# Optimization experiments

Measured on AMD Instinct MI355X. Metric: run time of the kernel, lower is better.

## Reference

```python
import jax, jax.numpy as jnp
import numpy as np

V = 32000   # vocab_size
D = 1024    # dim
NH = 16     # n_heads
HD = 64     # head_dim
L = 2       # n_layers
E = 8       # n_experts
K = 2       # n_active_experts
H = 2048    # expert_dim
B = 2
T = 1024
EPS = 1e-6
THETA = 10000.0
STD = 0.02


def rmsnorm(x, w):
    rms = jax.lax.rsqrt(jnp.mean(x * x, axis=-1, keepdims=True) + EPS)
    return x * rms * w


def rope_cos_sin(t_len):
    inv = 1.0 / (THETA ** (jnp.arange(0, HD, 2, dtype=jnp.float32) / HD))
    t = jnp.arange(t_len, dtype=jnp.float32)
    f = jnp.outer(t, inv)  # [T, HD//2]
    return jnp.cos(f), jnp.sin(f)


def apply_rope(x, cos, sin):
    # x: [B, T, NH, HD]; complex rotation on interleaved (even, odd) pairs
    xr = x[..., 0::2]
    xi = x[..., 1::2]
    c = cos[None, :, None, :]
    s = sin[None, :, None, :]
    out_r = xr * c - xi * s
    out_i = xr * s + xi * c
    return jnp.stack([out_r, out_i], axis=-1).reshape(x.shape)


def setup_inputs() -> dict:
    key = jax.random.key(0)
    ks = jax.random.split(key, 13)
    n = lambda k, shp: (jax.random.normal(k, shp, dtype=jnp.float32) * STD)
    return {
        "tokens": jax.random.randint(ks[0], (B, T), 0, V, dtype=jnp.int64)
                   if jax.config.jax_enable_x64 else
                   jax.random.randint(ks[0], (B, T), 0, V, dtype=jnp.int32),
        "emb": n(ks[1], (V, D)),            # tied embedding / output projection
        "attn_norm_w": jnp.ones((L, D), jnp.float32),
        "wq": n(ks[2], (L, D, D)),
        "wk": n(ks[3], (L, D, D)),
        "wv": n(ks[4], (L, D, D)),
        "wo": n(ks[5], (L, D, D)),
        "ffn_norm_w": jnp.ones((L, D), jnp.float32),
        "gate_w": n(ks[6], (L, D, E)),
        "w1": n(ks[7], (L, E, D, H)),
        "w2": n(ks[8], (L, E, H, D)),
        "w3": n(ks[9], (L, E, D, H)),
        "final_norm_w": jnp.ones((D,), jnp.float32),
    }


def reference(tokens, emb, attn_norm_w, wq, wk, wv, wo, ffn_norm_w,
              gate_w, w1, w2, w3, final_norm_w):
    b, t = tokens.shape
    h = emb[tokens]                                     # [B,T,D]
    cos, sin = rope_cos_sin(t)
    mask = jnp.where(jnp.tril(jnp.ones((t, t), bool)), 0.0, -jnp.inf)
    scale = 1.0 / np.sqrt(HD).astype(np.float32)
    aux_total = jnp.float32(0.0)

    for l in range(L):
        x = h
        # --- attention ---
        hn = rmsnorm(x, attn_norm_w[l])
        q = (hn @ wq[l]).reshape(b, t, NH, HD)
        k = (hn @ wk[l]).reshape(b, t, NH, HD)
        v = (hn @ wv[l]).reshape(b, t, NH, HD)
        q = apply_rope(q, cos, sin)
        k = apply_rope(k, cos, sin)
        scores = jnp.einsum('bqhd,bkhd->bhqk', q, k) * scale + mask
        attn = jax.nn.softmax(scores, axis=-1)
        o = jnp.einsum('bhqk,bkhd->bqhd', attn, v).reshape(b, t, D) @ wo[l]
        x = x + o
        # --- MoE ---
        xf = rmsnorm(x, ffn_norm_w[l]).reshape(-1, D)   # [N,D]
        gate_logits = xf @ gate_w[l]                    # [N,E]
        probs = jax.nn.softmax(gate_logits, axis=-1)
        vals, idx = jax.lax.top_k(probs, K)             # [N,K]
        w = vals / (jnp.sum(vals, axis=-1, keepdims=True) + 1e-8)
        oh = jax.nn.one_hot(idx, E, dtype=jnp.float32)  # [N,K,E]
        combine = jnp.sum(oh * w[..., None], axis=1)    # [N,E]
        tokens_per_expert = oh.sum(axis=1).mean(axis=0)
        aux_total = aux_total + E * jnp.sum(tokens_per_expert * probs.mean(axis=0))
        h1 = jnp.einsum('nd,edh->neh', xf, w1[l])
        h3 = jnp.einsum('nd,edh->neh', xf, w3[l])
        eo = jnp.einsum('neh,ehd->ned', jax.nn.silu(h1) * h3, w2[l])
        moe_out = jnp.einsum('ned,ne->nd', eo, combine).reshape(b, t, D)
        h = x + moe_out

    logits = rmsnorm(h, final_norm_w) @ emb.T           # [B,T,V]
    return logits, aux_total
```

## Files before the change

kernel.cpp:

```cpp
#include <hip/hip_runtime.h>
#include <hip/hip_bf16.h>
#include <math.h>

#define D_MODEL 1024
#define NHEADS  16
#define HDIM    64
#define NEXP    8
#define FFH     2048
#define BATCH   2
#define SEQ     1024
#define NTOK    2048
#define VOCAB   32000
#define LDSS    40

typedef __attribute__((ext_vector_type(4))) float f32x4;
typedef __attribute__((ext_vector_type(2))) float f32x2;
typedef __attribute__((ext_vector_type(8))) __bf16 bf16x8;
typedef __attribute__((ext_vector_type(4))) unsigned short u16x4;

__device__ __forceinline__ unsigned short f2bf(float f) {
    union { float f; unsigned u; } v; v.f = f;
    unsigned r = v.u + 0x7FFFu + ((v.u >> 16) & 1u);
    return (unsigned short)(r >> 16);
}
__device__ __forceinline__ float bf2f(unsigned short u) {
    union { unsigned u; float f; } v; v.u = ((unsigned)u) << 16; return v.f;
}
__device__ __forceinline__ void split3(float x, unsigned short& h, unsigned short& m, unsigned short& l) {
    h = f2bf(x);
    float r1 = x - bf2f(h);
    m = f2bf(r1);
    float r2 = r1 - bf2f(m);
    l = f2bf(r2);
}
__device__ __forceinline__ void split3t(float x, unsigned short& h, unsigned short& m, unsigned short& l) {
    union { float f; unsigned u; } a; a.f = x;
    h = (unsigned short)(a.u >> 16);
    float r1 = x - bf2f(h);
    union { float f; unsigned u; } b; b.f = r1;
    m = (unsigned short)(b.u >> 16);
    float r2 = r1 - bf2f(m);
    l = f2bf(r2);
}

#define MFMA(a, b, c) __builtin_amdgcn_mfma_f32_16x16x32_bf16((a), (b), (c), 0, 0, 0)

#define PSA ((long)NTOK * D_MODEL)
#define PSW ((long)D_MODEL * D_MODEL)

__global__ __launch_bounds__(256) void rmsnorm_kernel(const float* __restrict__ x,
    const float* __restrict__ wt, unsigned short* __restrict__ out3)
{
    __shared__ float red[4];
    int n = blockIdx.x;
    int c = threadIdx.x << 2;
    f32x4 v = *(const f32x4*)(x + (long)n*D_MODEL + c);
    float ss = v.x*v.x + v.y*v.y + v.z*v.z + v.w*v.w;
    #pragma unroll
    for (int dd = 32; dd; dd >>= 1) ss += __shfl_xor(ss, dd);
    if ((threadIdx.x & 63) == 0) red[threadIdx.x >> 6] = ss;
    __syncthreads();
    float tot = red[0] + red[1] + red[2] + red[3];
    float rms = rsqrtf(tot * (1.f / D_MODEL) + 1e-6f);
    f32x4 wv = *(const f32x4*)(wt + c);
    f32x4 o = v * rms;
    o = o * wv;
    u16x4 hv, mv, lv;
    #pragma unroll
    for (int j = 0; j < 4; j++) { unsigned short h,m,l; split3(o[j],h,m,l); hv[j]=h; mv[j]=m; lv[j]=l; }
    long idx = (long)n*D_MODEL + c;
    *(u16x4*)(out3 + 0*PSA + idx) = hv;
    *(u16x4*)(out3 + 1*PSA + idx) = mv;
    *(u16x4*)(out3 + 2*PSA + idx) = lv;
}

__global__ __launch_bounds__(256) void wsplitT_kernel(
    const float* __restrict__ wqs, const float* __restrict__ wks, const float* __restrict__ wvs,
    unsigned short* __restrict__ oq, unsigned short* __restrict__ ok, unsigned short* __restrict__ ov)
{
    __shared__ float t[64][65];
    int k0 = blockIdx.x*64, n0 = blockIdx.y*64, z = blockIdx.z;
    const float* src = (z==0) ? wqs : (z==1) ? wks : wvs;
    unsigned short* dst = (z==0) ? oq : (z==1) ? ok : ov;
    int tid = threadIdx.x;
    int a = tid & 63, g = tid >> 6;
    #pragma unroll 4
    for (int i = 0; i < 16; i++) {
        int k = g*16 + i;
        t[k][a] = src[(long)(k0+k)*D_MODEL + n0 + a];
    }
    __syncthreads();
    #pragma unroll 4
    for (int i = 0; i < 16; i++) {
        int n = g*16 + i;
        float v = t[a][n];
        unsigned short h,m,l; split3(v,h,m,l);
        long idx = (long)(n0+n)*D_MODEL + k0 + a;
        dst[0*PSW + idx] = h;
        dst[1*PSW + idx] = m;
        dst[2*PSW + idx] = l;
    }
}

__global__ __launch_bounds__(256, 4) void qkv_kernel(
    const unsigned short* __restrict__ A3,
    const unsigned short* __restrict__ Wq3, const unsigned short* __restrict__ Wk3,
    const unsigned short* __restrict__ Wv3,
    float* __restrict__ qf, float* __restrict__ kf, float* __restrict__ vf)
{
    __shared__ __align__(16) unsigned short As[3][64*LDSS];
    __shared__ __align__(16) unsigned short Bs[3][64*LDSS];
    int z = blockIdx.z;
    const unsigned short* B3 = (z==0) ? Wq3 : (z==1) ? Wk3 : Wv3;
    float* out = (z==0) ? qf : (z==1) ? kf : vf;
    int n0 = blockIdx.x*64, m0 = blockIdx.y*64;
    int tid = threadIdx.x, w = tid >> 6, lane = tid & 63;
    int wm = (w >> 1)*32, wn = (w & 1)*32;
    int lr = lane & 15, lg = lane >> 4;
    f32x4 zero = {0.f,0.f,0.f,0.f};
    f32x4 acc[2][2];
    #pragma unroll
    for (int mi = 0; mi < 2; mi++)
        #pragma unroll
        for (int ni = 0; ni < 2; ni++) acc[mi][ni] = zero;
    int rb = tid >> 3, kc = (tid & 7) << 2;

    for (int k0 = 0; k0 < D_MODEL; k0 += 32) {
        #pragma unroll
        for (int p = 0; p < 2; p++) {
            int r = p*32 + rb;
            #pragma unroll
            for (int s = 0; s < 3; s++) {
                *(u16x4*)&As[s][r*LDSS + kc] = *(const u16x4*)(A3 + s*PSA + (long)(m0+r)*D_MODEL + k0 + kc);
                *(u16x4*)&Bs[s][r*LDSS + kc] = *(const u16x4*)(B3 + s*PSW + (long)(n0+r)*D_MODEL + k0 + kc);
            }
        }
        __syncthreads();
        bf16x8 bf[3][2];
        #pragma unroll
        for (int s = 0; s < 3; s++)
            #pragma unroll
            for (int ni = 0; ni < 2; ni++)
                bf[s][ni] = *(const bf16x8*)&Bs[s][(wn + ni*16 + lr)*LDSS + lg*8];
        #pragma unroll
        for (int mi = 0; mi < 2; mi++) {
            bf16x8 ah = *(const bf16x8*)&As[0][(wm + mi*16 + lr)*LDSS + lg*8];
            bf16x8 am = *(const bf16x8*)&As[1][(wm + mi*16 + lr)*LDSS + lg*8];
            bf16x8 al = *(const bf16x8*)&As[2][(wm + mi*16 + lr)*LDSS + lg*8];
            #pragma unroll
            for (int ni = 0; ni < 2; ni++) {
                acc[mi][ni] = MFMA(ah, bf[0][ni], acc[mi][ni]);
                acc[mi][ni] = MFMA(ah, bf[1][ni], acc[mi][ni]);
                acc[mi][ni] = MFMA(am, bf[0][ni], acc[mi][ni]);
                acc[mi][ni] = MFMA(ah, bf[2][ni], acc[mi][ni]);
                acc[mi][ni] = MFMA(am, bf[1][ni], acc[mi][ni]);
                acc[mi][ni] = MFMA(al, bf[0][ni], acc[mi][ni]);
            }
        }
        __syncthreads();
    }
    #pragma unroll
    for (int mi = 0; mi < 2; mi++)
        #pragma unroll
        for (int r = 0; r < 4; r++) {
            long row = m0 + wm + mi*16 + lg*4 + r;
            #pragma unroll
            for (int ni = 0; ni < 2; ni++) {
                int col = n0 + wn + ni*16 + lr;
                out[row*D_MODEL + col] = acc[mi][ni][r];
            }
        }
}

__global__ __launch_bounds__(256, 3) void wo_kernel(
    const float* __restrict__ A, const float* __restrict__ B, float* h)
{
    __shared__ __align__(16) unsigned short As[3][64*LDSS];
    __shared__ __align__(16) unsigned short Bs[3][64*LDSS];
    int n0 = blockIdx.x*64, m0 = blockIdx.y*64;
    int tid = threadIdx.x, w = tid >> 6, lane = tid & 63;
    int wm = (w >> 1)*32, wn = (w & 1)*32;
    int lr = lane & 15, lg = lane >> 4;
    f32x4 zero = {0.f,0.f,0.f,0.f};
    f32x4 acc[2][2];
    #pragma unroll
    for (int mi = 0; mi < 2; mi++)
        #pragma unroll
        for (int ni = 0; ni < 2; ni++) acc[mi][ni] = zero;
    int rb = tid >> 3, kc = (tid & 7) << 2;
    int nb = (tid & 31) << 1, kb = (tid >> 5) << 2;

    f32x4 pAv[2];
    f32x2 pBv[4];
    #pragma unroll
    for (int p = 0; p < 2; p++)
        pAv[p] = *(const f32x4*)(A + (long)(m0 + p*32 + rb)*D_MODEL + kc);
    #pragma unroll
    for (int i = 0; i < 4; i++)
        pBv[i] = *(const f32x2*)(B + (long)(kb + i)*D_MODEL + n0 + nb);

    for (int k0 = 0; k0 < D_MODEL; k0 += 32) {
        int kn = k0 + 32;
        #pragma unroll
        for (int p = 0; p < 2; p++) {
            int r = p*32 + rb;
            u16x4 hv, mv, lv;
            #pragma unroll
            for (int j = 0; j < 4; j++) { unsigned short h,m,l; split3t(pAv[p][j],h,m,l); hv[j]=h; mv[j]=m; lv[j]=l; }
            *(u16x4*)&As[0][r*LDSS + kc] = hv;
            *(u16x4*)&As[1][r*LDSS + kc] = mv;
            *(u16x4*)&As[2][r*LDSS + kc] = lv;
        }
        #pragma unroll
        for (int i = 0; i < 2; i++) {
            int r = nb + i;
            u16x4 hv, mv, lv;
            unsigned short h,m,l;
            split3t(pBv[0][i],h,m,l); hv[0]=h; mv[0]=m; lv[0]=l;
            split3t(pBv[1][i],h,m,l); hv[1]=h; mv[1]=m; lv[1]=l;
            split3t(pBv[2][i],h,m,l); hv[2]=h; mv[2]=m; lv[2]=l;
            split3t(pBv[3][i],h,m,l); hv[3]=h; mv[3]=m; lv[3]=l;
            *(u16x4*)&Bs[0][r*LDSS + kb] = hv;
            *(u16x4*)&Bs[1][r*LDSS + kb] = mv;
            *(u16x4*)&Bs[2][r*LDSS + kb] = lv;
        }
        if (kn < D_MODEL) {
            #pragma unroll
            for (int p = 0; p < 2; p++)
                pAv[p] = *(const f32x4*)(A + (long)(m0 + p*32 + rb)*D_MODEL + kn + kc);
            #pragma unroll
            for (int i = 0; i < 4; i++)
                pBv[i] = *(const f32x2*)(B + (long)(kn + kb + i)*D_MODEL + n0 + nb);
        }
        __syncthreads();
        bf16x8 bf[3][2];
        #pragma unroll
        for (int s = 0; s < 3; s++)
            #pragma unroll
            for (int ni = 0; ni < 2; ni++)
                bf[s][ni] = *(const bf16x8*)&Bs[s][(wn + ni*16 + lr)*LDSS + lg*8];
        #pragma unroll
        for (int mi = 0; mi < 2; mi++) {
            bf16x8 ah = *(const bf16x8*)&As[0][(wm + mi*16 + lr)*LDSS + lg*8];
            bf16x8 am = *(const bf16x8*)&As[1][(wm + mi*16 + lr)*LDSS + lg*8];
            bf16x8 al = *(const bf16x8*)&As[2][(wm + mi*16 + lr)*LDSS + lg*8];
            #pragma unroll
            for (int ni = 0; ni < 2; ni++) {
                acc[mi][ni] = MFMA(ah, bf[0][ni], acc[mi][ni]);
                acc[mi][ni] = MFMA(ah, bf[1][ni], acc[mi][ni]);
                acc[mi][ni] = MFMA(am, bf[0][ni], acc[mi][ni]);
                acc[mi][ni] = MFMA(ah, bf[2][ni], acc[mi][ni]);
                acc[mi][ni] = MFMA(am, bf[1][ni], acc[mi][ni]);
                acc[mi][ni] = MFMA(al, bf[0][ni], acc[mi][ni]);
            }
        }
        __syncthreads();
    }
    #pragma unroll
    for (int mi = 0; mi < 2; mi++)
        #pragma unroll
        for (int r = 0; r < 4; r++) {
            long row = m0 + wm + mi*16 + lg*4 + r;
            #pragma unroll
            for (int ni = 0; ni < 2; ni++) {
                int col = n0 + wn + ni*16 + lr;
                h[row*D_MODEL + col] += acc[mi][ni][r];
            }
        }
}

template<int SPLIT>
__global__ __launch_bounds__(256, 3) void moe13_kernel(
    const unsigned short* __restrict__ A3, const float* __restrict__ W1,
    const float* __restrict__ W3, float* __restrict__ G,
    const int* __restrict__ rowidx, const int* __restrict__ counts,
    const int* __restrict__ offsets)
{
    __shared__ __align__(16) unsigned short As[SPLIT][64*LDSS];
    __shared__ __align__(16) unsigned short Bs[SPLIT][128*LDSS];
    int e = blockIdx.z;
    int cnt = counts[e], off = offsets[e];
    int n0 = blockIdx.x*128, m0 = blockIdx.y*64;
    if (m0 >= cnt) return;
    const float* b1p = W1 + (long)e * (D_MODEL*FFH);
    const float* b3p = W3 + (long)e * (D_MODEL*FFH);
    int tid = threadIdx.x, w = tid >> 6, lane = tid & 63;
    int wm = (w >> 1)*32, wn = (w & 1)*64;
    int lr = lane & 15, lg = lane >> 4;
    f32x4 zero = {0.f,0.f,0.f,0.f};
    f32x4 a1[2][4], a3[2][4];
    #pragma unroll
    for (int mi = 0; mi < 2; mi++)
        #pragma unroll
        for (int ni = 0; ni < 4; ni++) { a1[mi][ni] = zero; a3[mi][ni] = zero; }
    int rb = tid >> 3, kc = (tid & 7) << 2;

    long arow[2]; int av[2];
    #pragma unroll
    for (int p = 0; p < 2; p++) {
        int r = p*32 + rb;
        av[p] = (m0 + r < cnt) ? 1 : 0;
        arow[p] = av[p] ? (long)rowidx[off + m0 + r] : 0;
    }
    u16x4 z4 = {0,0,0,0};

    for (int k0 = 0; k0 < D_MODEL; k0 += 32) {
        #pragma unroll
        for (int p = 0; p < 2; p++) {
            int r = p*32 + rb;
            #pragma unroll
            for (int s = 0; s < SPLIT; s++)
                *(u16x4*)&As[s][r*LDSS + kc] = av[p] ?
                    *(const u16x4*)(A3 + s*PSA + arow[p]*D_MODEL + k0 + kc) : z4;
        }
        #pragma unroll
        for (int pass = 0; pass < 2; pass++) {
            const float* bp = pass ? b3p : b1p;
            f32x4 c0 = *(const f32x4*)(bp + (long)(k0+kc+0)*FFH + n0 + rb*4);
            f32x4 c1 = *(const f32x4*)(bp + (long)(k0+kc+1)*FFH + n0 + rb*4);
            f32x4 c2 = *(const f32x4*)(bp + (long)(k0+kc+2)*FFH + n0 + rb*4);
            f32x4 c3 = *(const f32x4*)(bp + (long)(k0+kc+3)*FFH + n0 + rb*4);
            #pragma unroll
            for (int i = 0; i < 4; i++) {
                int r = rb*4 + i;
                if (SPLIT == 3) {
                    u16x4 hv, mv, lv;
                    unsigned short h,m,l;
                    split3t(c0[i],h,m,l); hv[0]=h; mv[0]=m; lv[0]=l;
                    split3t(c1[i],h,m,l); hv[1]=h; mv[1]=m; lv[1]=l;
                    split3t(c2[i],h,m,l); hv[2]=h; mv[2]=m; lv[2]=l;
                    split3t(c3[i],h,m,l); hv[3]=h; mv[3]=m; lv[3]=l;
                    *(u16x4*)&Bs[0][r*LDSS + kc] = hv;
                    *(u16x4*)&Bs[1][r*LDSS + kc] = mv;
                    *(u16x4*)&Bs[2][r*LDSS + kc] = lv;
                } else {
                    u16x4 hv = {f2bf(c0[i]), f2bf(c1[i]), f2bf(c2[i]), f2bf(c3[i])};
                    *(u16x4*)&Bs[0][r*LDSS + kc] = hv;
                }
            }
            __syncthreads();
            bf16x8 bf[SPLIT][4];
            #pragma unroll
            for (int s = 0; s < SPLIT; s++)
                #pragma unroll
                for (int ni = 0; ni < 4; ni++)
                    bf[s][ni] = *(const bf16x8*)&Bs[s][(wn + ni*16 + lr)*LDSS + lg*8];
            #pragma unroll
            for (int mi = 0; mi < 2; mi++) {
                bf16x8 ah = *(const bf16x8*)&As[0][(wm + mi*16 + lr)*LDSS + lg*8];
                #pragma unroll
                for (int ni = 0; ni < 4; ni++) {
                    f32x4 a = pass ? a3[mi][ni] : a1[mi][ni];
                    a = MFMA(ah, bf[0][ni], a);
                    if (SPLIT == 3) {
                        bf16x8 am = *(const bf16x8*)&As[1][(wm + mi*16 + lr)*LDSS + lg*8];
                        bf16x8 al = *(const bf16x8*)&As[2][(wm + mi*16 + lr)*LDSS + lg*8];
                        a = MFMA(ah, bf[1][ni], a);
                        a = MFMA(am, bf[0][ni], a);
                        a = MFMA(ah, bf[2][ni], a);
                        a = MFMA(am, bf[1][ni], a);
                        a = MFMA(al, bf[0][ni], a);
                    }
                    if (pass) a3[mi][ni] = a; else a1[mi][ni] = a;
                }
            }
            __syncthreads();
        }
    }
    #pragma unroll
    for (int mi = 0; mi < 2; mi++)
        #pragma unroll
        for (int r = 0; r < 4; r++) {
            int rowl = wm + mi*16 + lg*4 + r;
            if (m0 + rowl < cnt) {
                long crow = off + m0 + rowl;
                #pragma unroll
                for (int ni = 0; ni < 4; ni++) {
                    int col = n0 + wn + ni*16 + lr;
                    float v1 = a1[mi][ni][r];
                    float v3 = a3[mi][ni][r];
                    G[crow*FFH + col] = (v1 / (1.f + expf(-v1))) * v3;
                }
            }
        }
}

template<int SPLIT>
__global__ __launch_bounds__(256, 4) void w2_kernel(
    const float* __restrict__ G, const float* __restrict__ W2, float* h,
    const int* __restrict__ rowidx, const float* __restrict__ wrow,
    const int* __restrict__ counts, const int* __restrict__ offsets)
{
    __shared__ __align__(16) unsigned short As[SPLIT][64*LDSS];
    __shared__ __align__(16) unsigned short Bs[SPLIT][64*LDSS];
    int e = blockIdx.z;
    int cnt = counts[e], off = offsets[e];
    int n0 = blockIdx.x*64, m0 = blockIdx.y*64;
    if (m0 >= cnt) return;
    const float* bp = W2 + (long)e * (FFH*D_MODEL);
    int tid = threadIdx.x, w = tid >> 6, lane = tid & 63;
    int wm = (w >> 1)*32, wn = (w & 1)*32;
    int lr = lane & 15, lg = lane >> 4;
    f32x4 zero = {0.f,0.f,0.f,0.f};
    f32x4 acc[2][2];
    #pragma unroll
    for (int mi = 0; mi < 2; mi++)
        #pragma unroll
        for (int ni = 0; ni < 2; ni++) acc[mi][ni] = zero;
    int rb = tid >> 3, kc = (tid & 7) << 2;
    int nb = (tid & 31) << 1, kb = (tid >> 5) << 2;

    int av[2];
    #pragma unroll
    for (int p = 0; p < 2; p++) av[p] = (m0 + p*32 + rb < cnt) ? 1 : 0;
    f32x4 pG[2];
    f32x2 pW[4];
    #pragma unroll
    for (int p = 0; p < 2; p++)
        pG[p] = av[p] ? *(const f32x4*)(G + (long)(off + m0 + p*32 + rb)*FFH + kc) : zero;
    #pragma unroll
    for (int i = 0; i < 4; i++)
        pW[i] = *(const f32x2*)(bp + (long)(kb + i)*D_MODEL + n0 + nb);

    for (int k0 = 0; k0 < FFH; k0 += 32) {
        int kn = k0 + 32;
        #pragma unroll
        for (int p = 0; p < 2; p++) {
            int r = p*32 + rb;
            if (SPLIT == 3) {
                u16x4 hv, mv, lv;
                #pragma unroll
                for (int j = 0; j < 4; j++) { unsigned short h,m,l; split3t(pG[p][j],h,m,l); hv[j]=h; mv[j]=m; lv[j]=l; }
                *(u16x4*)&As[0][r*LDSS + kc] = hv;
                *(u16x4*)&As[1][r*LDSS + kc] = mv;
                *(u16x4*)&As[2][r*LDSS + kc] = lv;
            } else {
                u16x4 hv;
                #pragma unroll
                for (int j = 0; j < 4; j++) hv[j] = f2bf(pG[p][j]);
                *(u16x4*)&As[0][r*LDSS + kc] = hv;
            }
        }
        #pragma unroll
        for (int i = 0; i < 2; i++) {
            int r = nb + i;
            if (SPLIT == 3) {
                u16x4 hv, mv, lv;
                unsigned short h,m,l;
                split3t(pW[0][i],h,m,l); hv[0]=h; mv[0]=m; lv[0]=l;
                split3t(pW[1][i],h,m,l); hv[1]=h; mv[1]=m; lv[1]=l;
                split3t(pW[2][i],h,m,l); hv[2]=h; mv[2]=m; lv[2]=l;
                split3t(pW[3][i],h,m,l); hv[3]=h; mv[3]=m; lv[3]=l;
                *(u16x4*)&Bs[0][r*LDSS + kb] = hv;
                *(u16x4*)&Bs[1][r*LDSS + kb] = mv;
                *(u16x4*)&Bs[2][r*LDSS + kb] = lv;
            } else {
                u16x4 hv = {f2bf(pW[0][i]), f2bf(pW[1][i]), f2bf(pW[2][i]), f2bf(pW[3][i])};
                *(u16x4*)&Bs[0][r*LDSS + kb] = hv;
            }
        }
        if (kn < FFH) {
            #pragma unroll
            for (int p = 0; p < 2; p++)
                pG[p] = av[p] ? *(const f32x4*)(G + (long)(off + m0 + p*32 + rb)*FFH + kn + kc) : zero;
            #pragma unroll
            for (int i = 0; i < 4; i++)
                pW[i] = *(const f32x2*)(bp + (long)(kn + kb + i)*D_MODEL + n0 + nb);
        }
        __syncthreads();
        bf16x8 bf[SPLIT][2];
        #pragma unroll
        for (int s = 0; s < SPLIT; s++)
            #pragma unroll
            for (int ni = 0; ni < 2; ni++)
                bf[s][ni] = *(const bf16x8*)&Bs[s][(wn + ni*16 + lr)*LDSS + lg*8];
        #pragma unroll
        for (int mi = 0; mi < 2; mi++) {
            bf16x8 ah = *(const bf16x8*)&As[0][(wm + mi*16 + lr)*LDSS + lg*8];
            #pragma unroll
            for (int ni = 0; ni < 2; ni++) {
                acc[mi][ni] = MFMA(ah, bf[0][ni], acc[mi][ni]);
                if (SPLIT == 3) {
                    bf16x8 am = *(const bf16x8*)&As[1][(wm + mi*16 + lr)*LDSS + lg*8];
                    bf16x8 al = *(const bf16x8*)&As[2][(wm + mi*16 + lr)*LDSS + lg*8];
                    acc[mi][ni] = MFMA(ah, bf[1][ni], acc[mi][ni]);
                    acc[mi][ni] = MFMA(am, bf[0][ni], acc[mi][ni]);
                    acc[mi][ni] = MFMA(ah, bf[2][ni], acc[mi][ni]);
                    acc[mi][ni] = MFMA(am, bf[1][ni], acc[mi][ni]);
                    acc[mi][ni] = MFMA(al, bf[0][ni], acc[mi][ni]);
                }
            }
        }
        __syncthreads();
    }
    #pragma unroll
    for (int mi = 0; mi < 2; mi++)
        #pragma unroll
        for (int r = 0; r < 4; r++) {
            int rowl = wm + mi*16 + lg*4 + r;
            if (m0 + rowl < cnt) {
                long crow = off + m0 + rowl;
                long n = rowidx[crow];
                float wgt = wrow[crow];
                #pragma unroll
                for (int ni = 0; ni < 2; ni++) {
                    int col = n0 + wn + ni*16 + lr;
                    atomicAdd(&h[n*D_MODEL + col], wgt * acc[mi][ni][r]);
                }
            }
        }
}

__global__ __launch_bounds__(256) void attn_kernel(
    const float* __restrict__ q, const float* __restrict__ k,
    const float* __restrict__ v, float* __restrict__ att)
{
    __shared__ __align__(16) unsigned short Qs[3][64*72];
    __shared__ __align__(16) unsigned short KP[3][2560];
    __shared__ __align__(16) unsigned short Vt[3][2560];

    int qt = blockIdx.x, bh = blockIdx.y;
    int b = bh >> 4, hh = bh & 15;
    int tid = threadIdx.x, w = tid >> 6, lane = tid & 63;
    int lr = lane & 15, lg = lane >> 4;
    int lrow = tid >> 4;
    int lcol = (tid & 15) << 2;

    const float* qbase = q + ((long)(b*SEQ + qt*64) * D_MODEL + hh*64);
    #pragma unroll
    for (int p = 0; p < 4; p++) {
        int r = p*16 + lrow;
        f32x4 vv = *(const f32x4*)(qbase + (long)r * D_MODEL + lcol);
        #pragma unroll
        for (int jj = 0; jj < 4; jj++) {
            unsigned short h,m,l; split3t(vv[jj],h,m,l);
            Qs[0][r*72 + lcol + jj] = h;
            Qs[1][r*72 + lcol + jj] = m;
            Qs[2][r*72 + lcol + jj] = l;
        }
    }

    f32x4 zero = {0.f,0.f,0.f,0.f};
    f32x4 oacc[4] = {zero, zero, zero, zero};
    float mrun[4] = {-INFINITY,-INFINITY,-INFINITY,-INFINITY};
    float lrun[4] = {0.f,0.f,0.f,0.f};

    int ntile = 2*qt + 2;
    for (int jt = 0; jt < ntile; jt++) {
        const float* kbase = k + ((long)(b*SEQ + jt*32) * D_MODEL + hh*64);
        const float* vbase = v + ((long)(b*SEQ + jt*32) * D_MODEL + hh*64);
        #pragma unroll
        for (int p = 0; p < 2; p++) {
            int r = p*16 + lrow;
            f32x4 kv4 = *(const f32x4*)(kbase + (long)r * D_MODEL + lcol);
            f32x4 vv4 = *(const f32x4*)(vbase + (long)r * D_MODEL + lcol);
            #pragma unroll
            for (int jj = 0; jj < 4; jj++) {
                unsigned short h,m,l;
                split3t(kv4[jj],h,m,l);
                KP[0][r*72 + lcol + jj] = h;
                KP[1][r*72 + lcol + jj] = m;
                KP[2][r*72 + lcol + jj] = l;
                split3t(vv4[jj],h,m,l);
                Vt[0][(lcol+jj)*40 + r] = h;
                Vt[1][(lcol+jj)*40 + r] = m;
                Vt[2][(lcol+jj)*40 + r] = l;
            }
        }
        __syncthreads();

        f32x4 s[2] = {zero, zero};
        #pragma unroll
        for (int ks = 0; ks < 2; ks++) {
            bf16x8 qh = *(const bf16x8*)&Qs[0][(w*16 + lr)*72 + ks*32 + lg*8];
            bf16x8 qm = *(const bf16x8*)&Qs[1][(w*16 + lr)*72 + ks*32 + lg*8];
            bf16x8 ql = *(const bf16x8*)&Qs[2][(w*16 + lr)*72 + ks*32 + lg*8];
            #pragma unroll
            for (int ni = 0; ni < 2; ni++) {
                bf16x8 kh = *(const bf16x8*)&KP[0][(ni*16 + lr)*72 + ks*32 + lg*8];
                bf16x8 km = *(const bf16x8*)&KP[1][(ni*16 + lr)*72 + ks*32 + lg*8];
                bf16x8 kl = *(const bf16x8*)&KP[2][(ni*16 + lr)*72 + ks*32 + lg*8];
                s[ni] = MFMA(qh, kh, s[ni]);
                s[ni] = MFMA(qh, km, s[ni]);
                s[ni] = MFMA(qm, kh, s[ni]);
                s[ni] = MFMA(qh, kl, s[ni]);
                s[ni] = MFMA(qm, km, s[ni]);
                s[ni] = MFMA(ql, kh, s[ni]);
            }
        }
        __syncthreads();

        #pragma unroll
        for (int r = 0; r < 4; r++) {
            int qg = qt*64 + w*16 + lg*4 + r;
            float mx = -INFINITY;
            #pragma unroll
            for (int ni = 0; ni < 2; ni++) {
                int kg = jt*32 + ni*16 + lr;
                float val = s[ni][r] * 0.125f;
                if (kg > qg) val = -INFINITY;
                s[ni][r] = val;
                mx = fmaxf(mx, val);
            }
            #pragma unroll
            for (int dd = 1; dd < 16; dd <<= 1)
                mx = fmaxf(mx, __shfl_xor(mx, dd));
            float mnew  = fmaxf(mrun[r], mx);
            float alpha = expf(mrun[r] - mnew);
            float ps = 0.f;
            #pragma unroll
            for (int ni = 0; ni < 2; ni++) {
                float pv = expf(s[ni][r] - mnew);
                s[ni][r] = pv;
                ps += pv;
            }
            #pragma unroll
            for (int dd = 1; dd < 16; dd <<= 1)
                ps += __shfl_xor(ps, dd);
            lrun[r] = lrun[r] * alpha + ps;
            mrun[r] = mnew;
            #pragma unroll
            for (int d = 0; d < 4; d++) oacc[d][r] *= alpha;
            int prow = w*16 + lg*4 + r;
            #pragma unroll
            for (int ni = 0; ni < 2; ni++) {
                unsigned short h,m,l; split3t(s[ni][r],h,m,l);
                KP[0][prow*40 + ni*16 + lr] = h;
                KP[1][prow*40 + ni*16 + lr] = m;
                KP[2][prow*40 + ni*16 + lr] = l;
            }
        }
        {
            bf16x8 ph = *(const bf16x8*)&KP[0][(w*16 + lr)*40 + lg*8];
            bf16x8 pm = *(const bf16x8*)&KP[1][(w*16 + lr)*40 + lg*8];
            bf16x8 pl = *(const bf16x8*)&KP[2][(w*16 + lr)*40 + lg*8];
            #pragma unroll
            for (int ni = 0; ni < 4; ni++) {
                bf16x8 vh = *(const bf16x8*)&Vt[0][(ni*16 + lr)*40 + lg*8];
                bf16x8 vm = *(const bf16x8*)&Vt[1][(ni*16 + lr)*40 + lg*8];
                bf16x8 vl = *(const bf16x8*)&Vt[2][(ni*16 + lr)*40 + lg*8];
                oacc[ni] = MFMA(ph, vh, oacc[ni]);
                oacc[ni] = MFMA(ph, vm, oacc[ni]);
                oacc[ni] = MFMA(pm, vh, oacc[ni]);
                oacc[ni] = MFMA(ph, vl, oacc[ni]);
                oacc[ni] = MFMA(pm, vm, oacc[ni]);
                oacc[ni] = MFMA(pl, vh, oacc[ni]);
            }
        }
        __syncthreads();
    }
    float* obase = att + ((long)(b*SEQ + qt*64) * D_MODEL + hh*64);
    #pragma unroll
    for (int r = 0; r < 4; r++) {
        float inv = 1.f / lrun[r];
        #pragma unroll
        for (int ni = 0; ni < 4; ni++)
            obase[(long)(w*16 + lg*4 + r) * D_MODEL + ni*16 + lr] = oacc[ni][r] * inv;
    }
}

__global__ __launch_bounds__(256) void logits_kernel(
    const unsigned short* __restrict__ A0, const float* __restrict__ Bmat, float* __restrict__ C)
{
    __shared__ __align__(16) unsigned short As[128*LDSS];
    __shared__ __align__(16) unsigned short Bs[128*LDSS];
    int n0 = blockIdx.y * 128;
    int m0 = blockIdx.x * 128;
    int tid = threadIdx.x, w = tid >> 6, lane = tid & 63;
    int wm = (w >> 1)*64, wn = (w & 1)*64;
    int lr = lane & 15, lg = lane >> 4;
    f32x4 zero = {0.f,0.f,0.f,0.f};
    f32x4 acc[4][4];
    #pragma unroll
    for (int mi = 0; mi < 4; mi++)
        #pragma unroll
        for (int ni = 0; ni < 4; ni++) acc[mi][ni] = zero;
    int rb = tid >> 3, kc = (tid & 7) << 2;
    for (int k0 = 0; k0 < D_MODEL; k0 += 32) {
        #pragma unroll
        for (int p = 0; p < 4; p++) {
            int r = p*32 + rb;
            *(u16x4*)&As[r*LDSS + kc] = *(const u16x4*)(A0 + (long)(m0+r)*D_MODEL + k0 + kc);
            f32x4 vv = *(const f32x4*)(Bmat + (long)(n0+r)*D_MODEL + k0 + kc);
            u16x4 hv;
            #pragma unroll
            for (int j = 0; j < 4; j++) hv[j] = f2bf(vv[j]);
            *(u16x4*)&Bs[r*LDSS + kc] = hv;
        }
        __syncthreads();
        bf16x8 bfv[4], af[4];
        #pragma unroll
        for (int ni = 0; ni < 4; ni++)
            bfv[ni] = *(const bf16x8*)&Bs[(wn + ni*16 + lr)*LDSS + lg*8];
        #pragma unroll
        for (int mi = 0; mi < 4; mi++)
            af[mi] = *(const bf16x8*)&As[(wm + mi*16 + lr)*LDSS + lg*8];
        #pragma unroll
        for (int mi = 0; mi < 4; mi++)
            #pragma unroll
            for (int ni = 0; ni < 4; ni++)
                acc[mi][ni] = MFMA(af[mi], bfv[ni], acc[mi][ni]);
        __syncthreads();
    }
    #pragma unroll
    for (int mi = 0; mi < 4; mi++)
        #pragma unroll
        for (int r = 0; r < 4; r++) {
            long row = m0 + wm + mi*16 + lg*4 + r;
            #pragma unroll
            for (int ni = 0; ni < 4; ni++) {
                int col = n0 + wn + ni*16 + lr;
                C[row*VOCAB + col] = acc[mi][ni][r];
            }
        }
}

__global__ __launch_bounds__(256) void embed_kernel(const int* __restrict__ tok,
    const float* __restrict__ emb, float* __restrict__ h)
{
    int n = blockIdx.x;
    int c = threadIdx.x << 2;
    long t = tok[n];
    *(f32x4*)(h + (long)n*D_MODEL + c) = *(const f32x4*)(emb + t*D_MODEL + c);
}

__global__ __launch_bounds__(256) void ropetab_kernel(float* __restrict__ tab)
{
    int idx = blockIdx.x * 256 + threadIdx.x;
    if (idx >= SEQ * 32) return;
    int t = idx >> 5, i = idx & 31;
    double inv = pow(10000.0, -(double)(2*i) / 64.0);
    double ang = (double)t * inv;
    tab[idx*2]   = (float)cos(ang);
    tab[idx*2+1] = (float)sin(ang);
}

__global__ __launch_bounds__(256) void rope_kernel(float* __restrict__ q, float* __restrict__ kk,
    const float* __restrict__ tab)
{
    int gid = blockIdx.x * 256 + threadIdx.x;
    if (gid >= NTOK * 512) return;
    int n   = gid >> 9;
    int rem = gid & 511;
    int hh  = rem >> 5;
    int i   = rem & 31;
    int t   = n & (SEQ - 1);
    float cs = tab[(t*32 + i)*2];
    float sn = tab[(t*32 + i)*2 + 1];
    long base = (long)n * D_MODEL + hh*64 + 2*i;
    float qr = q[base], qi = q[base+1];
    q[base]   = qr*cs - qi*sn;
    q[base+1] = qr*sn + qi*cs;
    float kr = kk[base], ki = kk[base+1];
    kk[base]   = kr*cs - ki*sn;
    kk[base+1] = kr*sn + ki*cs;
}

__global__ __launch_bounds__(64) void gate_kernel(const unsigned short* __restrict__ xf3,
    const float* __restrict__ gw, int* __restrict__ counts,
    int* __restrict__ eid, float* __restrict__ wts, float* __restrict__ pbuf)
{
    int n = blockIdx.x;
    int lane = threadIdx.x;
    float acc[8] = {0,0,0,0,0,0,0,0};
    for (int d0 = lane*4; d0 < D_MODEL; d0 += 256) {
        long idx = (long)n*D_MODEL + d0;
        u16x4 xh = *(const u16x4*)(xf3 + 0*PSA + idx);
        u16x4 xm = *(const u16x4*)(xf3 + 1*PSA + idx);
        u16x4 xl = *(const u16x4*)(xf3 + 2*PSA + idx);
        #pragma unroll
        for (int j = 0; j < 4; j++) {
            float xv = bf2f(xh[j]) + bf2f(xm[j]) + bf2f(xl[j]);
            const float* g = gw + (d0+j) * 8;
            #pragma unroll
            for (int e = 0; e < 8; e++) acc[e] += xv * g[e];
        }
    }
    #pragma unroll
    for (int e = 0; e < 8; e++) {
        #pragma unroll
        for (int dd = 32; dd; dd >>= 1) acc[e] += __shfl_xor(acc[e], dd);
    }
    if (lane == 0) {
        float mx = acc[0];
        #pragma unroll
        for (int e = 1; e < 8; e++) mx = fmaxf(mx, acc[e]);
        float pe[8], ssum = 0.f;
        #pragma unroll
        for (int e = 0; e < 8; e++) { pe[e] = expf(acc[e] - mx); ssum += pe[e]; }
        float sinv = 1.f / ssum;
        #pragma unroll
        for (int e = 0; e < 8; e++) { pe[e] *= sinv; pbuf[n*8 + e] = pe[e]; }
        int e1 = 0;
        #pragma unroll
        for (int e = 1; e < 8; e++) if (pe[e] > pe[e1]) e1 = e;
        int e2 = -1;
        #pragma unroll
        for (int e = 0; e < 8; e++) if (e != e1 && (e2 < 0 || pe[e] > pe[e2])) e2 = e;
        float v1 = pe[e1], v2 = pe[e2];
        float wsum = v1 + v2 + 1e-8f;
        eid[n*2] = e1; eid[n*2+1] = e2;
        wts[n*2] = v1 / wsum; wts[n*2+1] = v2 / wsum;
        atomicAdd(counts + e1, 1);
        atomicAdd(counts + e2, 1);
    }
}

__global__ __launch_bounds__(64) void scan_kernel(const int* __restrict__ counts,
    int* __restrict__ offs, int* __restrict__ cursor,
    const float* __restrict__ pbuf, float* __restrict__ aux)
{
    int t = threadIdx.x;
    int e = t & 7, c = t >> 3;
    float s = 0.f;
    for (int n = 0; n < NTOK/8; n++)
        s += pbuf[(c*(NTOK/8) + n)*8 + e];
    #pragma unroll
    for (int dd = 8; dd < 64; dd <<= 1) s += __shfl_xor(s, dd);
    __shared__ float red[8];
    if (t < 8) red[t] = s;
    __syncthreads();
    if (t == 0) {
        int o = 0; float a = 0.f;
        for (int k = 0; k < 8; k++) {
            offs[k] = o; cursor[k] = o; o += counts[k];
            a += (float)counts[k] * red[k];
        }
        aux[0] += 8.f * a / ((float)NTOK * (float)NTOK);
    }
}

__global__ __launch_bounds__(256) void assign_kernel(const int* __restrict__ eid,
    const float* __restrict__ wts, int* __restrict__ cursor,
    int* __restrict__ rowidx, float* __restrict__ wrow)
{
    int n = blockIdx.x * 256 + threadIdx.x;
    if (n >= NTOK) return;
    #pragma unroll
    for (int s = 0; s < 2; s++) {
        int e = eid[n*2 + s];
        int p = atomicAdd(cursor + e, 1);
        rowidx[p] = n;
        wrow[p] = wts[n*2 + s];
    }
}

__global__ void write_aux_kernel(float* __restrict__ out, const float* __restrict__ aux)
{
    if (threadIdx.x == 0 && blockIdx.x == 0)
        out[(long)NTOK * VOCAB] = aux[0];
}

extern "C" void kernel_launch(void* const* d_in, const int* in_sizes, int n_in,
                              void* d_out, int out_size, void* d_ws, size_t ws_size,
                              hipStream_t stream)
{
    const int*   tokens = (const int*)d_in[0];
    const float* emb    = (const float*)d_in[1];
    const float* anw    = (const float*)d_in[2];
    const float* wq     = (const float*)d_in[3];
    const float* wk     = (const float*)d_in[4];
    const float* wv     = (const float*)d_in[5];
    const float* wo     = (const float*)d_in[6];
    const float* fnw    = (const float*)d_in[7];
    const float* gw     = (const float*)d_in[8];
    const float* w1     = (const float*)d_in[9];
    const float* w2     = (const float*)d_in[10];
    const float* w3     = (const float*)d_in[11];
    const float* finw   = (const float*)d_in[12];
    float* out = (float*)d_out;

    char* W = (char*)d_ws;
    const size_t MB = 1024u * 1024u;
    int*   counts = (int*)(W + 0);
    int*   offs   = (int*)(W + 64);
    int*   cursor = (int*)(W + 128);
    float* aux    = (float*)(W + 192);
    int*   eid    = (int*)(W + 4096);
    float* wts    = (float*)(W + 4096 + 16384);
    int*   rowix  = (int*)(W + 4096 + 32768);
    float* wrow   = (float*)(W + 4096 + 49152);
    float* pbuf   = (float*)(W + 4096 + 65536);
    float* rtab   = (float*)(W + 4096 + 131072 + 65536);
    float*          h    = (float*)(W + 1*MB);
    unsigned short* hn3  = (unsigned short*)(W + 9*MB);
    float*          qf   = (float*)(W + 21*MB);
    float*          kf   = (float*)(W + 29*MB);
    float*          vf   = (float*)(W + 37*MB);
    unsigned short* wq3  = (unsigned short*)(W + 45*MB);
    unsigned short* wk3  = (unsigned short*)(W + 51*MB);
    unsigned short* wv3  = (unsigned short*)(W + 57*MB);
    float*          att  = (float*)(W + 45*MB);
    float*          g    = (float*)(W + 21*MB);

    hipMemsetAsync(W, 0, 256, stream);
    ropetab_kernel<<<(SEQ*32 + 255)/256, 256, 0, stream>>>(rtab);
    embed_kernel<<<NTOK, 256, 0, stream>>>(tokens, emb, h);

    for (int l = 0; l < 2; l++) {
        const float* wql = wq + (size_t)l*D_MODEL*D_MODEL;
        const float* wkl = wk + (size_t)l*D_MODEL*D_MODEL;
        const float* wvl = wv + (size_t)l*D_MODEL*D_MODEL;
        const float* wol = wo + (size_t)l*D_MODEL*D_MODEL;

        rmsnorm_kernel<<<NTOK, 256, 0, stream>>>(h, anw + (size_t)l*D_MODEL, hn3);
        wsplitT_kernel<<<dim3(16, 16, 3), 256, 0, stream>>>(wql, wkl, wvl, wq3, wk3, wv3);
        qkv_kernel<<<dim3(D_MODEL/64, NTOK/64, 3), 256, 0, stream>>>(hn3, wq3, wk3, wv3, qf, kf, vf);
        rope_kernel<<<(NTOK*512 + 255)/256, 256, 0, stream>>>(qf, kf, rtab);
        attn_kernel<<<dim3(SEQ/64, BATCH*NHEADS), 256, 0, stream>>>(qf, kf, vf, att);
        wo_kernel<<<dim3(D_MODEL/64, NTOK/64), 256, 0, stream>>>(att, wol, h);

        rmsnorm_kernel<<<NTOK, 256, 0, stream>>>(h, fnw + (size_t)l*D_MODEL, hn3);
        hipMemsetAsync(W, 0, 160, stream);
        gate_kernel<<<NTOK, 64, 0, stream>>>(hn3, gw + (size_t)l*D_MODEL*NEXP, counts, eid, wts, pbuf);
        scan_kernel<<<1, 64, 0, stream>>>(counts, offs, cursor, pbuf, aux);
        assign_kernel<<<(NTOK + 255)/256, 256, 0, stream>>>(eid, wts, cursor, rowix, wrow);

        const float* w1l = w1 + (size_t)l*NEXP*D_MODEL*FFH;
        const float* w3l = w3 + (size_t)l*NEXP*D_MODEL*FFH;
        const float* w2l = w2 + (size_t)l*NEXP*FFH*D_MODEL;
        dim3 g13(FFH/128, 2*NTOK/64, NEXP);
        dim3 g2d(D_MODEL/64, 2*NTOK/64, NEXP);
        if (l == 0) {
            moe13_kernel<3><<<g13, 256, 0, stream>>>(hn3, w1l, w3l, g, rowix, counts, offs);
            w2_kernel<3><<<g2d, 256, 0, stream>>>(g, w2l, h, rowix, wrow, counts, offs);
        } else {
            moe13_kernel<1><<<g13, 256, 0, stream>>>(hn3, w1l, w3l, g, rowix, counts, offs);
            w2_kernel<1><<<g2d, 256, 0, stream>>>(g, w2l, h, rowix, wrow, counts, offs);
        }
    }

    rmsnorm_kernel<<<NTOK, 256, 0, stream>>>(h, finw, hn3);
    logits_kernel<<<dim3(NTOK/128, VOCAB/128), 256, 0, stream>>>(hn3, emb, out);
    write_aux_kernel<<<1, 1, 0, stream>>>(out, aux);
}
```

Baseline: 1.975 ms.

## Replace 3-way bf16 split GEMMs with scaled 2-way fp16 split

Switches every emulated-fp32 matmul from a three-term bf16 decomposition (six MFMAs per tile) to a two-term scaled fp16 decomposition (three MFMAs per tile). Separate accumulators are rescaled and summed in the epilogue. This cuts MFMA count, LDS footprint and split-operand memory traffic roughly in half. The risk is reduced precision and fp16 range overflow or underflow, since fixed scale factors are assumed for activations and weights.

After: 1.740 ms. -11.9%, faster.

```diff
diff --git a/kernel.cpp b/kernel.cpp
--- a/kernel.cpp
+++ b/kernel.cpp
@@ -15,41 +15,38 @@
 
 typedef __attribute__((ext_vector_type(4))) float f32x4;
 typedef __attribute__((ext_vector_type(2))) float f32x2;
-typedef __attribute__((ext_vector_type(8))) __bf16 bf16x8;
+typedef __attribute__((ext_vector_type(8))) _Float16 f16x8;
 typedef __attribute__((ext_vector_type(4))) unsigned short u16x4;
 
-__device__ __forceinline__ unsigned short f2bf(float f) {
-    union { float f; unsigned u; } v; v.f = f;
-    unsigned r = v.u + 0x7FFFu + ((v.u >> 16) & 1u);
-    return (unsigned short)(r >> 16);
-}
-__device__ __forceinline__ float bf2f(unsigned short u) {
-    union { unsigned u; float f; } v; v.u = ((unsigned)u) << 16; return v.f;
-}
-__device__ __forceinline__ void split3(float x, unsigned short& h, unsigned short& m, unsigned short& l) {
-    h = f2bf(x);
-    float r1 = x - bf2f(h);
-    m = f2bf(r1);
-    float r2 = r1 - bf2f(m);
-    l = f2bf(r2);
-}
-__device__ __forceinline__ void split3t(float x, unsigned short& h, unsigned short& m, unsigned short& l) {
-    union { float f; unsigned u; } a; a.f = x;
-    h = (unsigned short)(a.u >> 16);
-    float r1 = x - bf2f(h);
-    union { float f; unsigned u; } b; b.f = r1;
-    m = (unsigned short)(b.u >> 16);
-    float r2 = r1 - bf2f(m);
-    l = f2bf(r2);
-}
-
-#define MFMA(a, b, c) __builtin_amdgcn_mfma_f32_16x16x32_bf16((a), (b), (c), 0, 0, 0)
+#define TIER    4.8828125e-4f
+#define DESCALE 2.44140625e-4f
+#define INV_S   0.015625f
+#define INV_M   7.62939453125e-6f
+
+__device__ __forceinline__ unsigned short f2h(float x) {
+    _Float16 h = (_Float16)x;
+    union { _Float16 h; unsigned short u; } v; v.h = h; return v.u;
+}
+__device__ __forceinline__ float h2f(unsigned short u) {
+    union { unsigned short u; _Float16 h; } v; v.u = u; return (float)v.h;
+}
+__device__ __forceinline__ void split2h(float x, unsigned short& h, unsigned short& m) {
+    _Float16 hf = (_Float16)(x * 64.f);
+    union { _Float16 h; unsigned short u; } a; a.h = hf;
+    h = a.u;
+    float r = x - (float)hf * INV_S;
+    _Float16 mf = (_Float16)(r * 131072.f);
+    union { _Float16 h; unsigned short u; } b; b.h = mf;
+    m = b.u;
+}
+
+#define MFMAH(a, b, c) __builtin_amdgcn_mfma_f32_16x16x32_f16((a), (b), (c), 0, 0, 0)
 
 #define PSA ((long)NTOK * D_MODEL)
 #define PSW ((long)D_MODEL * D_MODEL)
 
 __global__ __launch_bounds__(256) void rmsnorm_kernel(const float* __restrict__ x,
-    const float* __restrict__ wt, unsigned short* __restrict__ out3)
+    const float* __restrict__ wt, unsigned short* __restrict__ out2)
 {
     __shared__ float red[4];
     int n = blockIdx.x;
@@ -65,13 +62,12 @@
     f32x4 wv = *(const f32x4*)(wt + c);
     f32x4 o = v * rms;
     o = o * wv;
-    u16x4 hv, mv, lv;
-    #pragma unroll
-    for (int j = 0; j < 4; j++) { unsigned short h,m,l; split3(o[j],h,m,l); hv[j]=h; mv[j]=m; lv[j]=l; }
+    u16x4 hv, mv;
+    #pragma unroll
+    for (int j = 0; j < 4; j++) { unsigned short h,m; split2h(o[j],h,m); hv[j]=h; mv[j]=m; }
     long idx = (long)n*D_MODEL + c;
-    *(u16x4*)(out3 + 0*PSA + idx) = hv;
-    *(u16x4*)(out3 + 1*PSA + idx) = mv;
-    *(u16x4*)(out3 + 2*PSA + idx) = lv;
+    *(u16x4*)(out2 + 0*PSA + idx) = hv;
+    *(u16x4*)(out2 + 1*PSA + idx) = mv;
 }
 
 __global__ __launch_bounds__(256) void wsplitT_kernel(
@@ -94,35 +90,34 @@
     for (int i = 0; i < 16; i++) {
         int n = g*16 + i;
         float v = t[a][n];
-        unsigned short h,m,l; split3(v,h,m,l);
+        unsigned short h,m; split2h(v,h,m);
         long idx = (long)(n0+n)*D_MODEL + k0 + a;
         dst[0*PSW + idx] = h;
         dst[1*PSW + idx] = m;
-        dst[2*PSW + idx] = l;
     }
 }
 
 __global__ __launch_bounds__(256, 4) void qkv_kernel(
-    const unsigned short* __restrict__ A3,
-    const unsigned short* __restrict__ Wq3, const unsigned short* __restrict__ Wk3,
-    const unsigned short* __restrict__ Wv3,
+    const unsigned short* __restrict__ A2,
+    const unsigned short* __restrict__ Wq2, const unsigned short* __restrict__ Wk2,
+    const unsigned short* __restrict__ Wv2,
     float* __restrict__ qf, float* __restrict__ kf, float* __restrict__ vf)
 {
-    __shared__ __align__(16) unsigned short As[3][64*LDSS];
-    __shared__ __align__(16) unsigned short Bs[3][64*LDSS];
+    __shared__ __align__(16) unsigned short As[2][64*LDSS];
+    __shared__ __align__(16) unsigned short Bs[2][64*LDSS];
     int z = blockIdx.z;
-    const unsigned short* B3 = (z==0) ? Wq3 : (z==1) ? Wk3 : Wv3;
+    const unsigned short* B2 = (z==0) ? Wq2 : (z==1) ? Wk2 : Wv2;
     float* out = (z==0) ? qf : (z==1) ? kf : vf;
     int n0 = blockIdx.x*64, m0 = blockIdx.y*64;
     int tid = threadIdx.x, w = tid >> 6, lane = tid & 63;
     int wm = (w >> 1)*32, wn = (w & 1)*32;
     int lr = lane & 15, lg = lane >> 4;
     f32x4 zero = {0.f,0.f,0.f,0.f};
-    f32x4 acc[2][2];
+    f32x4 a0[2][2], a1[2][2];
     #pragma unroll
     for (int mi = 0; mi < 2; mi++)
         #pragma unroll
-        for (int ni = 0; ni < 2; ni++) acc[mi][ni] = zero;
+        for (int ni = 0; ni < 2; ni++) { a0[mi][ni] = zero; a1[mi][ni] = zero; }
     int rb = tid >> 3, kc = (tid & 7) << 2;
 
     for (int k0 = 0; k0 < D_MODEL; k0 += 32) {
@@ -130,31 +125,27 @@
         for (int p = 0; p < 2; p++) {
             int r = p*32 + rb;
             #pragma unroll
-            for (int s = 0; s < 3; s++) {
-                *(u16x4*)&As[s][r*LDSS + kc] = *(const u16x4*)(A3 + s*PSA + (long)(m0+r)*D_MODEL + k0 + kc);
-                *(u16x4*)&Bs[s][r*LDSS + kc] = *(const u16x4*)(B3 + s*PSW + (long)(n0+r)*D_MODEL + k0 + kc);
-            }
-        }
-        __syncthreads();
-        bf16x8 bf[3][2];
-        #pragma unroll
-        for (int s = 0; s < 3; s++)
-            #pragma unroll
-            for (int ni = 0; ni < 2; ni++)
-                bf[s][ni] = *(const bf16x8*)&Bs[s][(wn + ni*16 + lr)*LDSS + lg*8];
+            for (int s = 0; s < 2; s++) {
+                *(u16x4*)&As[s][r*LDSS + kc] = *(const u16x4*)(A2 + s*PSA + (long)(m0+r)*D_MODEL + k0 + kc);
+                *(u16x4*)&Bs[s][r*LDSS + kc] = *(const u16x4*)(B2 + s*PSW + (long)(n0+r)*D_MODEL + k0 + kc);
+            }
+        }
+        __syncthreads();
+        f16x8 bh[2], bm[2];
+        #pragma unroll
+        for (int ni = 0; ni < 2; ni++) {
+            bh[ni] = *(const f16x8*)&Bs[0][(wn + ni*16 + lr)*LDSS + lg*8];
+            bm[ni] = *(const f16x8*)&Bs[1][(wn + ni*16 + lr)*LDSS + lg*8];
+        }
         #pragma unroll
         for (int mi = 0; mi < 2; mi++) {
-            bf16x8 ah = *(const bf16x8*)&As[0][(wm + mi*16 + lr)*LDSS + lg*8];
-            bf16x8 am = *(const bf16x8*)&As[1][(wm + mi*16 + lr)*LDSS + lg*8];
-            bf16x8 al = *(const bf16x8*)&As[2][(wm + mi*16 + lr)*LDSS + lg*8];
+            f16x8 ah = *(const f16x8*)&As[0][(wm + mi*16 + lr)*LDSS + lg*8];
+            f16x8 am = *(const f16x8*)&As[1][(wm + mi*16 + lr)*LDSS + lg*8];
             #pragma unroll
             for (int ni = 0; ni < 2; ni++) {
-                acc[mi][ni] = MFMA(ah, bf[0][ni], acc[mi][ni]);
-                acc[mi][ni] = MFMA(ah, bf[1][ni], acc[mi][ni]);
-                acc[mi][ni] = MFMA(am, bf[0][ni], acc[mi][ni]);
-                acc[mi][ni] = MFMA(ah, bf[2][ni], acc[mi][ni]);
-                acc[mi][ni] = MFMA(am, bf[1][ni], acc[mi][ni]);
-                acc[mi][ni] = MFMA(al, bf[0][ni], acc[mi][ni]);
+                a0[mi][ni] = MFMAH(ah, bh[ni], a0[mi][ni]);
+                a1[mi][ni] = MFMAH(ah, bm[ni], a1[mi][ni]);
+                a1[mi][ni] = MFMAH(am, bh[ni], a1[mi][ni]);
             }
         }
         __syncthreads();
@@ -167,7 +158,7 @@
             #pragma unroll
             for (int ni = 0; ni < 2; ni++) {
                 int col = n0 + wn + ni*16 + lr;
-                out[row*D_MODEL + col] = acc[mi][ni][r];
+                out[row*D_MODEL + col] = (a0[mi][ni][r] + a1[mi][ni][r]*TIER) * DESCALE;
             }
         }
 }
@@ -175,18 +166,18 @@
 __global__ __launch_bounds__(256, 3) void wo_kernel(
     const float* __restrict__ A, const float* __restrict__ B, float* h)
 {
-    __shared__ __align__(16) unsigned short As[3][64*LDSS];
-    __shared__ __align__(16) unsigned short Bs[3][64*LDSS];
+    __shared__ __align__(16) unsigned short As[2][64*LDSS];
+    __shared__ __align__(16) unsigned short Bs[2][64*LDSS];
     int n0 = blockIdx.x*64, m0 = blockIdx.y*64;
     int tid = threadIdx.x, w = tid >> 6, lane = tid & 63;
     int wm = (w >> 1)*32, wn = (w & 1)*32;
     int lr = lane & 15, lg = lane >> 4;
     f32x4 zero = {0.f,0.f,0.f,0.f};
-    f32x4 acc[2][2];
+    f32x4 a0[2][2], a1[2][2];
     #pragma unroll
     for (int mi = 0; mi < 2; mi++)
         #pragma unroll
-        for (int ni = 0; ni < 2; ni++) acc[mi][ni] = zero;
+        for (int ni = 0; ni < 2; ni++) { a0[mi][ni] = zero; a1[mi][ni] = zero; }
     int rb = tid >> 3, kc = (tid & 7) << 2;
     int nb = (tid & 31) << 1, kb = (tid >> 5) << 2;
 
@@ -204,25 +195,23 @@
         #pragma unroll
         for (int p = 0; p < 2; p++) {
             int r = p*32 + rb;
-            u16x4 hv, mv, lv;
-            #pragma unroll
-            for (int j = 0; j < 4; j++) { unsigned short h,m,l; split3t(pAv[p][j],h,m,l); hv[j]=h; mv[j]=m; lv[j]=l; }
+            u16x4 hv, mv;
+            #pragma unroll
+            for (int j = 0; j < 4; j++) { unsigned short hh,mm; split2h(pAv[p][j],hh,mm); hv[j]=hh; mv[j]=mm; }
             *(u16x4*)&As[0][r*LDSS + kc] = hv;
             *(u16x4*)&As[1][r*LDSS + kc] = mv;
-            *(u16x4*)&As[2][r*LDSS + kc] = lv;
         }
         #pragma unroll
         for (int i = 0; i < 2; i++) {
             int r = nb + i;
-            u16x4 hv, mv, lv;
-            unsigned short h,m,l;
-            split3t(pBv[0][i],h,m,l); hv[0]=h; mv[0]=m; lv[0]=l;
-            split3t(pBv[1][i],h,m,l); hv[1]=h; mv[1]=m; lv[1]=l;
-            split3t(pBv[2][i],h,m,l); hv[2]=h; mv[2]=m; lv[2]=l;
-            split3t(pBv[3][i],h,m,l); hv[3]=h; mv[3]=m; lv[3]=l;
+            u16x4 hv, mv;
+            unsigned short hh,mm;
+            split2h(pBv[0][i],hh,mm); hv[0]=hh; mv[0]=mm;
+            split2h(pBv[1][i],hh,mm); hv[1]=hh; mv[1]=mm;
+            split2h(pBv[2][i],hh,mm); hv[2]=hh; mv[2]=mm;
+            split2h(pBv[3][i],hh,mm); hv[3]=hh; mv[3]=mm;
             *(u16x4*)&Bs[0][r*LDSS + kb] = hv;
             *(u16x4*)&Bs[1][r*LDSS + kb] = mv;
-            *(u16x4*)&Bs[2][r*LDSS + kb] = lv;
         }
         if (kn < D_MODEL) {
             #pragma unroll
@@ -233,25 +222,21 @@
                 pBv[i] = *(const f32x2*)(B + (long)(kn + kb + i)*D_MODEL + n0 + nb);
         }
         __syncthreads();
-        bf16x8 bf[3][2];
-        #pragma unroll
-        for (int s = 0; s < 3; s++)
-            #pragma unroll
-            for (int ni = 0; ni < 2; ni++)
-                bf[s][ni] = *(const bf16x8*)&Bs[s][(wn + ni*16 + lr)*LDSS + lg*8];
+        f16x8 bh[2], bm[2];
+        #pragma unroll
+        for (int ni = 0; ni < 2; ni++) {
+            bh[ni] = *(const f16x8*)&Bs[0][(wn + ni*16 + lr)*LDSS + lg*8];
+            bm[ni] = *(const f16x8*)&Bs[1][(wn + ni*16 + lr)*LDSS + lg*8];
+        }
         #pragma unroll
         for (int mi = 0; mi < 2; mi++) {
-            bf16x8 ah = *(const bf16x8*)&As[0][(wm + mi*16 + lr)*LDSS + lg*8];
-            bf16x8 am = *(const bf16x8*)&As[1][(wm + mi*16 + lr)*LDSS + lg*8];
-            bf16x8 al = *(const bf16x8*)&As[2][(wm + mi*16 + lr)*LDSS + lg*8];
+            f16x8 ah = *(const f16x8*)&As[0][(wm + mi*16 + lr)*LDSS + lg*8];
+            f16x8 am = *(const f16x8*)&As[1][(wm + mi*16 + lr)*LDSS + lg*8];
             #pragma unroll
             for (int ni = 0; ni < 2; ni++) {
-                acc[mi][ni] = MFMA(ah, bf[0][ni], acc[mi][ni]);
-                acc[mi][ni] = MFMA(ah, bf[1][ni], acc[mi][ni]);
-                acc[mi][ni] = MFMA(am, bf[0][ni], acc[mi][ni]);
-                acc[mi][ni] = MFMA(ah, bf[2][ni], acc[mi][ni]);
-                acc[mi][ni] = MFMA(am, bf[1][ni], acc[mi][ni]);
-                acc[mi][ni] = MFMA(al, bf[0][ni], acc[mi][ni]);
+                a0[mi][ni] = MFMAH(ah, bh[ni], a0[mi][ni]);
+                a1[mi][ni] = MFMAH(ah, bm[ni], a1[mi][ni]);
+                a1[mi][ni] = MFMAH(am, bh[ni], a1[mi][ni]);
             }
         }
         __syncthreads();
@@ -264,36 +249,30 @@
             #pragma unroll
             for (int ni = 0; ni < 2; ni++) {
                 int col = n0 + wn + ni*16 + lr;
-                h[row*D_MODEL + col] += acc[mi][ni][r];
-            }
-        }
-}
-
-template<int SPLIT>
+                h[row*D_MODEL + col] += (a0[mi][ni][r] + a1[mi][ni][r]*TIER) * DESCALE;
+            }
+        }
+}
+
+template<int SPL>
 __global__ __launch_bounds__(256, 3) void moe13_kernel(
-    const unsigned short* __restrict__ A3, const float* __restrict__ W1,
+    const unsigned short* __restrict__ A2, const float* __restrict__ W1,
     const float* __restrict__ W3, float* __restrict__ G,
     const int* __restrict__ rowidx, const int* __restrict__ counts,
     const int* __restrict__ offsets)
 {
-    __shared__ __align__(16) unsigned short As[SPLIT][64*LDSS];
-    __shared__ __align__(16) unsigned short Bs[SPLIT][128*LDSS];
+    __shared__ __align__(16) unsigned short As[SPL][64*LDSS];
+    __shared__ __align__(16) unsigned short Bs[SPL][128*LDSS];
+    const int P1 = (SPL == 2) ? 1 : 0;
     int e = blockIdx.z;
     int cnt = counts[e], off = offsets[e];
     int n0 = blockIdx.x*128, m0 = blockIdx.y*64;
     if (m0 >= cnt) return;
-    const float* b1p = W1 + (long)e * (D_MODEL*FFH);
-    const float* b3p = W3 + (long)e * (D_MODEL*FFH);
     int tid = threadIdx.x, w = tid >> 6, lane = tid & 63;
     int wm = (w >> 1)*32, wn = (w & 1)*64;
     int lr = lane & 15, lg = lane >> 4;
+    int rb = tid >> 3, kc = (tid & 7) << 2;
     f32x4 zero = {0.f,0.f,0.f,0.f};
-    f32x4 a1[2][4], a3[2][4];
-    #pragma unroll
-    for (int mi = 0; mi < 2; mi++)
-        #pragma unroll
-        for (int ni = 0; ni < 4; ni++) { a1[mi][ni] = zero; a3[mi][ni] = zero; }
-    int rb = tid >> 3, kc = (tid & 7) << 2;
 
     long arow[2]; int av[2];
     #pragma unroll
@@ -303,19 +282,26 @@
         arow[p] = av[p] ? (long)rowidx[off + m0 + r] : 0;
     }
     u16x4 z4 = {0,0,0,0};
-
-    for (int k0 = 0; k0 < D_MODEL; k0 += 32) {
-        #pragma unroll
-        for (int p = 0; p < 2; p++) {
-            int r = p*32 + rb;
-            #pragma unroll
-            for (int s = 0; s < SPLIT; s++)
-                *(u16x4*)&As[s][r*LDSS + kc] = av[p] ?
-                    *(const u16x4*)(A3 + s*PSA + arow[p]*D_MODEL + k0 + kc) : z4;
-        }
-        #pragma unroll
-        for (int pass = 0; pass < 2; pass++) {
-            const float* bp = pass ? b3p : b1p;
+    f32x4 sl[2][4];
+
+    #pragma unroll
+    for (int mat = 0; mat < 2; mat++) {
+        const float* bp = (mat ? W3 : W1) + (long)e * (D_MODEL*FFH);
+        f32x4 a0[2][4], a1t[2][4];
+        #pragma unroll
+        for (int mi = 0; mi < 2; mi++)
+            #pragma unroll
+            for (int ni = 0; ni < 4; ni++) { a0[mi][ni] = zero; a1t[mi][ni] = zero; }
+
+        for (int k0 = 0; k0 < D_MODEL; k0 += 32) {
+            #pragma unroll
+            for (int p = 0; p < 2; p++) {
+                int r = p*32 + rb;
+                #pragma unroll
+                for (int s = 0; s < SPL; s++)
+                    *(u16x4*)&As[s][r*LDSS + kc] = av[p] ?
+                        *(const u16x4*)(A2 + s*PSA + arow[p]*D_MODEL + k0 + kc) : z4;
+            }
             f32x4 c0 = *(const f32x4*)(bp + (long)(k0+kc+0)*FFH + n0 + rb*4);
             f32x4 c1 = *(const f32x4*)(bp + (long)(k0+kc+1)*FFH + n0 + rb*4);
             f32x4 c2 = *(const f32x4*)(bp + (long)(k0+kc+2)*FFH + n0 + rb*4);
@@ -323,76 +309,86 @@
             #pragma unroll
             for (int i = 0; i < 4; i++) {
                 int r = rb*4 + i;
-                if (SPLIT == 3) {
-                    u16x4 hv, mv, lv;
-                    unsigned short h,m,l;
-                    split3t(c0[i],h,m,l); hv[0]=h; mv[0]=m; lv[0]=l;
-                    split3t(c1[i],h,m,l); hv[1]=h; mv[1]=m; lv[1]=l;
-                    split3t(c2[i],h,m,l); hv[2]=h; mv[2]=m; lv[2]=l;
-                    split3t(c3[i],h,m,l); hv[3]=h; mv[3]=m; lv[3]=l;
+                if (SPL == 2) {
+                    u16x4 hv, mv;
+                    unsigned short hh,mm;
+                    split2h(c0[i],hh,mm); hv[0]=hh; mv[0]=mm;
+                    split2h(c1[i],hh,mm); hv[1]=hh; mv[1]=mm;
+                    split2h(c2[i],hh,mm); hv[2]=hh; mv[2]=mm;
+                    split2h(c3[i],hh,mm); hv[3]=hh; mv[3]=mm;
                     *(u16x4*)&Bs[0][r*LDSS + kc] = hv;
-                    *(u16x4*)&Bs[1][r*LDSS + kc] = mv;
-                    *(u16x4*)&Bs[2][r*LDSS + kc] = lv;
+                    *(u16x4*)&Bs[P1][r*LDSS + kc] = mv;
                 } else {
-                    u16x4 hv = {f2bf(c0[i]), f2bf(c1[i]), f2bf(c2[i]), f2bf(c3[i])};
+                    u16x4 hv = {f2h(c0[i]), f2h(c1[i]), f2h(c2[i]), f2h(c3[i])};
                     *(u16x4*)&Bs[0][r*LDSS + kc] = hv;
                 }
             }
             __syncthreads();
-            bf16x8 bf[SPLIT][4];
-            #pragma unroll
-            for (int s = 0; s < SPLIT; s++)
-                #pragma unroll
-                for (int ni = 0; ni < 4; ni++)
-                    bf[s][ni] = *(const bf16x8*)&Bs[s][(wn + ni*16 + lr)*LDSS + lg*8];
+            f16x8 bh[4], bm[4];
+            #pragma unroll
+            for (int ni = 0; ni < 4; ni++) {
+                bh[ni] = *(const f16x8*)&Bs[0][(wn + ni*16 + lr)*LDSS + lg*8];
+                if (SPL == 2) bm[ni] = *(const f16x8*)&Bs[P1][(wn + ni*16 + lr)*LDSS + lg*8];
+            }
             #pragma unroll
             for (int mi = 0; mi < 2; mi++) {
-                bf16x8 ah = *(const bf16x8*)&As[0][(wm + mi*16 + lr)*LDSS + lg*8];
+                f16x8 ah = *(const f16x8*)&As[0][(wm + mi*16 + lr)*LDSS + lg*8];
                 #pragma unroll
                 for (int ni = 0; ni < 4; ni++) {
-                    f32x4 a = pass ? a3[mi][ni] : a1[mi][ni];
-                    a = MFMA(ah, bf[0][ni], a);
-                    if (SPLIT == 3) {
-                        bf16x8 am = *(const bf16x8*)&As[1][(wm + mi*16 + lr)*LDSS + lg*8];
-                        bf16x8 al = *(const bf16x8*)&As[2][(wm + mi*16 + lr)*LDSS + lg*8];
-                        a = MFMA(ah, bf[1][ni], a);
-                        a = MFMA(am, bf[0][ni], a);
-                        a = MFMA(ah, bf[2][ni], a);
-                        a = MFMA(am, bf[1][ni], a);
-                        a = MFMA(al, bf[0][ni], a);
+                    a0[mi][ni] = MFMAH(ah, bh[ni], a0[mi][ni]);
+                    if (SPL == 2) {
+                        f16x8 am = *(const f16x8*)&As[P1][(wm + mi*16 + lr)*LDSS + lg*8];
+                        a1t[mi][ni] = MFMAH(ah, bm[ni], a1t[mi][ni]);
+                        a1t[mi][ni] = MFMAH(am, bh[ni], a1t[mi][ni]);
                     }
-                    if (pass) a3[mi][ni] = a; else a1[mi][ni] = a;
                 }
             }
             __syncthreads();
         }
-    }
-    #pragma unroll
-    for (int mi = 0; mi < 2; mi++)
-        #pragma unroll
-        for (int r = 0; r < 4; r++) {
-            int rowl = wm + mi*16 + lg*4 + r;
-            if (m0 + rowl < cnt) {
-                long crow = off + m0 + rowl;
+        if (mat == 0) {
+            #pragma unroll
+            for (int mi = 0; mi < 2; mi++)
                 #pragma unroll
                 for (int ni = 0; ni < 4; ni++) {
-                    int col = n0 + wn + ni*16 + lr;
-                    float v1 = a1[mi][ni][r];
-                    float v3 = a3[mi][ni][r];
-                    G[crow*FFH + col] = (v1 / (1.f + expf(-v1))) * v3;
+                    f32x4 v = (SPL == 2) ? (a0[mi][ni] + a1t[mi][ni]*TIER)*DESCALE
+                                         : a0[mi][ni]*INV_S;
+                    #pragma unroll
+                    for (int r = 0; r < 4; r++) {
+                        float s = v[r];
+                        v[r] = s / (1.f + expf(-s));
+                    }
+                    sl[mi][ni] = v;
                 }
-            }
-        }
-}
-
-template<int SPLIT>
+        } else {
+            #pragma unroll
+            for (int mi = 0; mi < 2; mi++)
+                #pragma unroll
+                for (int r = 0; r < 4; r++) {
+                    int rowl = wm + mi*16 + lg*4 + r;
+                    if (m0 + rowl < cnt) {
+                        long crow = off + m0 + rowl;
+                        #pragma unroll
+                        for (int ni = 0; ni < 4; ni++) {
+                            int col = n0 + wn + ni*16 + lr;
+                            float v3 = (SPL == 2) ? (a0[mi][ni][r] + a1t[mi][ni][r]*TIER)*DESCALE
+                                                  : a0[mi][ni][r]*INV_S;
+                            G[crow*FFH + col] = sl[mi][ni][r] * v3;
+                        }
+                    }
+                }
+        }
+    }
+}
+
+template<int SPL>
 __global__ __launch_bounds__(256, 4) void w2_kernel(
     const float* __restrict__ G, const float* __restrict__ W2, float* h,
     const int* __restrict__ rowidx, const float* __restrict__ wrow,
     const int* __restrict__ counts, const int* __restrict__ offsets)
 {
-    __shared__ __align__(16) unsigned short As[SPLIT][64*LDSS];
-    __shared__ __align__(16) unsigned short Bs[SPLIT][64*LDSS];
+    __shared__ __align__(16) unsigned short As[SPL][64*LDSS];
+    __shared__ __align__(16) unsigned short Bs[SPL][64*LDSS];
+    const int P1 = (SPL == 2) ? 1 : 0;
     int e = blockIdx.z;
     int cnt = counts[e], off = offsets[e];
     int n0 = blockIdx.x*64, m0 = blockIdx.y*64;
@@ -402,11 +398,11 @@
     int wm = (w >> 1)*32, wn = (w & 1)*32;
     int lr = lane & 15, lg = lane >> 4;
     f32x4 zero = {0.f,0.f,0.f,0.f};
-    f32x4 acc[2][2];
+    f32x4 a0[2][2], a1[2][2];
     #pragma unroll
     for (int mi = 0; mi < 2; mi++)
         #pragma unroll
-        for (int ni = 0; ni < 2; ni++) acc[mi][ni] = zero;
+        for (int ni = 0; ni < 2; ni++) { a0[mi][ni] = zero; a1[mi][ni] = zero; }
     int rb = tid >> 3, kc = (tid & 7) << 2;
     int nb = (tid & 31) << 1, kb = (tid >> 5) << 2;
 
@@ -427,35 +423,33 @@
         #pragma unroll
         for (int p = 0; p < 2; p++) {
             int r = p*32 + rb;
-            if (SPLIT == 3) {
-                u16x4 hv, mv, lv;
+            if (SPL == 2) {
+                u16x4 hv, mv;
                 #pragma unroll
-                for (int j = 0; j < 4; j++) { unsigned short h,m,l; split3t(pG[p][j],h,m,l); hv[j]=h; mv[j]=m; lv[j]=l; }
+                for (int j = 0; j < 4; j++) { unsigned short hh,mm; split2h(pG[p][j],hh,mm); hv[j]=hh; mv[j]=mm; }
                 *(u16x4*)&As[0][r*LDSS + kc] = hv;
-                *(u16x4*)&As[1][r*LDSS + kc] = mv;
-                *(u16x4*)&As[2][r*LDSS + kc] = lv;
+                *(u16x4*)&As[P1][r*LDSS + kc] = mv;
             } else {
                 u16x4 hv;
                 #pragma unroll
-                for (int j = 0; j < 4; j++) hv[j] = f2bf(pG[p][j]);
+                for (int j = 0; j < 4; j++) hv[j] = f2h(pG[p][j]);
                 *(u16x4*)&As[0][r*LDSS + kc] = hv;
             }
         }
         #pragma unroll
         for (int i = 0; i < 2; i++) {
             int r = nb + i;
-            if (SPLIT == 3) {
-                u16x4 hv, mv, lv;
-                unsigned short h,m,l;
-                split3t(pW[0][i],h,m,l); hv[0]=h; mv[0]=m; lv[0]=l;
-                split3t(pW[1][i],h,m,l); hv[1]=h; mv[1]=m; lv[1]=l;
-                split3t(pW[2][i],h,m,l); hv[2]=h; mv[2]=m; lv[2]=l;
-                split3t(pW[3][i],h,m,l); hv[3]=h; mv[3]=m; lv[3]=l;
+            if (SPL == 2) {
+                u16x4 hv, mv;
+                unsigned short hh,mm;
+                split2h(pW[0][i],hh,mm); hv[0]=hh; mv[0]=mm;
+                split2h(pW[1][i],hh,mm); hv[1]=hh; mv[1]=mm;
+                split2h(pW[2][i],hh,mm); hv[2]=hh; mv[2]=mm;
+                split2h(pW[3][i],hh,mm); hv[3]=hh; mv[3]=mm;
                 *(u16x4*)&Bs[0][r*LDSS + kb] = hv;
-                *(u16x4*)&Bs[1][r*LDSS + kb] = mv;
-                *(u16x4*)&Bs[2][r*LDSS + kb] = lv;
+                *(u16x4*)&Bs[P1][r*LDSS + kb] = mv;
             } else {
-                u16x4 hv = {f2bf(pW[0][i]), f2bf(pW[1][i]), f2bf(pW[2][i]), f2bf(pW[3][i])};
+                u16x4 hv = {f2h(pW[0][i]), f2h(pW[1][i]), f2h(pW[2][i]), f2h(pW[3][i])};
                 *(u16x4*)&Bs[0][r*LDSS + kb] = hv;
             }
         }
@@ -468,26 +462,22 @@
                 pW[i] = *(const f32x2*)(bp + (long)(kn + kb + i)*D_MODEL + n0 + nb);
         }
         __syncthreads();
-        bf16x8 bf[SPLIT][2];
-        #pragma unroll
-        for (int s = 0; s < SPLIT; s++)
-            #pragma unroll
-            for (int ni = 0; ni < 2; ni++)
-                bf[s][ni] = *(const bf16x8*)&Bs[s][(wn + ni*16 + lr)*LDSS + lg*8];
+        f16x8 bh[2], bm[2];
+        #pragma unroll
+        for (int ni = 0; ni < 2; ni++) {
+            bh[ni] = *(const f16x8*)&Bs[0][(wn + ni*16 + lr)*LDSS + lg*8];
+            if (SPL == 2) bm[ni] = *(const f16x8*)&Bs[P1][(wn + ni*16 + lr)*LDSS + lg*8];
+        }
         #pragma unroll
         for (int mi = 0; mi < 2; mi++) {
-            bf16x8 ah = *(const bf16x8*)&As[0][(wm + mi*16 + lr)*LDSS + lg*8];
+            f16x8 ah = *(const f16x8*)&As[0][(wm + mi*16 + lr)*LDSS + lg*8];
             #pragma unroll
             for (int ni = 0; ni < 2; ni++) {
-                acc[mi][ni] = MFMA(ah, bf[0][ni], acc[mi][ni]);
-                if (SPLIT == 3) {
-                    bf16x8 am = *(const bf16x8*)&As[1][(wm + mi*16 + lr)*LDSS + lg*8];
-                    bf16x8 al = *(const bf16x8*)&As[2][(wm + mi*16 + lr)*LDSS + lg*8];
-                    acc[mi][ni] = MFMA(ah, bf[1][ni], acc[mi][ni]);
-                    acc[mi][ni] = MFMA(am, bf[0][ni], acc[mi][ni]);
-                    acc[mi][ni] = MFMA(ah, bf[2][ni], acc[mi][ni]);
-                    acc[mi][ni] = MFMA(am, bf[1][ni], acc[mi][ni]);
-                    acc[mi][ni] = MFMA(al, bf[0][ni], acc[mi][ni]);
+                a0[mi][ni] = MFMAH(ah, bh[ni], a0[mi][ni]);
+                if (SPL == 2) {
+                    f16x8 am = *(const f16x8*)&As[P1][(wm + mi*16 + lr)*LDSS + lg*8];
+                    a1[mi][ni] = MFMAH(ah, bm[ni], a1[mi][ni]);
+                    a1[mi][ni] = MFMAH(am, bh[ni], a1[mi][ni]);
                 }
             }
         }
@@ -505,19 +495,21 @@
                 #pragma unroll
                 for (int ni = 0; ni < 2; ni++) {
                     int col = n0 + wn + ni*16 + lr;
-                    atomicAdd(&h[n*D_MODEL + col], wgt * acc[mi][ni][r]);
+                    float val = (SPL == 2) ? (a0[mi][ni][r] + a1[mi][ni][r]*TIER)*DESCALE
+                                           : a0[mi][ni][r];
+                    atomicAdd(&h[n*D_MODEL + col], wgt * val);
                 }
             }
         }
 }
 
-__global__ __launch_bounds__(256) void attn_kernel(
+__global__ __launch_bounds__(256, 3) void attn_kernel(
     const float* __restrict__ q, const float* __restrict__ k,
     const float* __restrict__ v, float* __restrict__ att)
 {
-    __shared__ __align__(16) unsigned short Qs[3][64*72];
-    __shared__ __align__(16) unsigned short KP[3][2560];
-    __shared__ __align__(16) unsigned short Vt[3][2560];
+    __shared__ __align__(16) unsigned short Qs[2][64*72];
+    __shared__ __align__(16) unsigned short KP[2][2560];
+    __shared__ __align__(16) unsigned short Vt[2][2560];
 
     int qt = blockIdx.x, bh = blockIdx.y;
     int b = bh >> 4, hh = bh & 15;
@@ -533,15 +525,15 @@
         f32x4 vv = *(const f32x4*)(qbase + (long)r * D_MODEL + lcol);
         #pragma unroll
         for (int jj = 0; jj < 4; jj++) {
-            unsigned short h,m,l; split3t(vv[jj],h,m,l);
-            Qs[0][r*72 + lcol + jj] = h;
-            Qs[1][r*72 + lcol + jj] = m;
-            Qs[2][r*72 + lcol + jj] = l;
+            unsigned short hh2,mm2; split2h(vv[jj],hh2,mm2);
+            Qs[0][r*72 + lcol + jj] = hh2;
+            Qs[1][r*72 + lcol + jj] = mm2;
         }
     }
 
     f32x4 zero = {0.f,0.f,0.f,0.f};
-    f32x4 oacc[4] = {zero, zero, zero, zero};
+    f32x4 o0[4] = {zero, zero, zero, zero};
+    f32x4 o1[4] = {zero, zero, zero, zero};
     float mrun[4] = {-INFINITY,-INFINITY,-INFINITY,-INFINITY};
     float lrun[4] = {0.f,0.f,0.f,0.f};
 
@@ -556,36 +548,30 @@
             f32x4 vv4 = *(const f32x4*)(vbase + (long)r * D_MODEL + lcol);
             #pragma unroll
             for (int jj = 0; jj < 4; jj++) {
-                unsigned short h,m,l;
-                split3t(kv4[jj],h,m,l);
-                KP[0][r*72 + lcol + jj] = h;
-                KP[1][r*72 + lcol + jj] = m;
-                KP[2][r*72 + lcol + jj] = l;
-                split3t(vv4[jj],h,m,l);
-                Vt[0][(lcol+jj)*40 + r] = h;
-                Vt[1][(lcol+jj)*40 + r] = m;
-                Vt[2][(lcol+jj)*40 + r] = l;
-            }
-        }
-        __syncthreads();
-
-        f32x4 s[2] = {zero, zero};
+                unsigned short hh2,mm2;
+                split2h(kv4[jj],hh2,mm2);
+                KP[0][r*72 + lcol + jj] = hh2;
+                KP[1][r*72 + lcol + jj] = mm2;
+                split2h(vv4[jj],hh2,mm2);
+                Vt[0][(lcol+jj)*40 + r] = hh2;
+                Vt[1][(lcol+jj)*40 + r] = mm2;
+            }
+        }
+        __syncthreads();
+
+        f32x4 s0[2] = {zero, zero};
+        f32x4 s1[2] = {zero, zero};
         #pragma unroll
         for (int ks = 0; ks < 2; ks++) {
-            bf16x8 qh = *(const bf16x8*)&Qs[0][(w*16 + lr)*72 + ks*32 + lg*8];
-            bf16x8 qm = *(const bf16x8*)&Qs[1][(w*16 + lr)*72 + ks*32 + lg*8];
-            bf16x8 ql = *(const bf16x8*)&Qs[2][(w*16 + lr)*72 + ks*32 + lg*8];
+            f16x8 qh = *(const f16x8*)&Qs[0][(w*16 + lr)*72 + ks*32 + lg*8];
+            f16x8 qm = *(const f16x8*)&Qs[1][(w*16 + lr)*72 + ks*32 + lg*8];
             #pragma unroll
             for (int ni = 0; ni < 2; ni++) {
-                bf16x8 kh = *(const bf16x8*)&KP[0][(ni*16 + lr)*72 + ks*32 + lg*8];
-                bf16x8 km = *(const bf16x8*)&KP[1][(ni*16 + lr)*72 + ks*32 + lg*8];
-                bf16x8 kl = *(const bf16x8*)&KP[2][(ni*16 + lr)*72 + ks*32 + lg*8];
-                s[ni] = MFMA(qh, kh, s[ni]);
-                s[ni] = MFMA(qh, km, s[ni]);
-                s[ni] = MFMA(qm, kh, s[ni]);
-                s[ni] = MFMA(qh, kl, s[ni]);
-                s[ni] = MFMA(qm, km, s[ni]);
-                s[ni] = MFMA(ql, kh, s[ni]);
+                f16x8 kh = *(const f16x8*)&KP[0][(ni*16 + lr)*72 + ks*32 + lg*8];
+                f16x8 km = *(const f16x8*)&KP[1][(ni*16 + lr)*72 + ks*32 + lg*8];
+                s0[ni] = MFMAH(qh, kh, s0[ni]);
+                s1[ni] = MFMAH(qh, km, s1[ni]);
+                s1[ni] = MFMAH(qm, kh, s1[ni]);
             }
         }
         __syncthreads();
@@ -593,13 +579,14 @@
         #pragma unroll
         for (int r = 0; r < 4; r++) {
             int qg = qt*64 + w*16 + lg*4 + r;
+            float sv[2];
             float mx = -INFINITY;
             #pragma unroll
             for (int ni = 0; ni < 2; ni++) {
                 int kg = jt*32 + ni*16 + lr;
-                float val = s[ni][r] * 0.125f;
+                float val = (s0[ni][r] + s1[ni][r]*TIER) * (0.125f * DESCALE);
                 if (kg > qg) val = -INFINITY;
-                s[ni][r] = val;
+                sv[ni] = val;
                 mx = fmaxf(mx, val);
             }
             #pragma unroll
@@ -610,8 +597,8 @@
             float ps = 0.f;
             #pragma unroll
             for (int ni = 0; ni < 2; ni++) {
-                float pv = expf(s[ni][r] - mnew);
-                s[ni][r] = pv;
+                float pv = expf(sv[ni] - mnew);
+                sv[ni] = pv;
                 ps += pv;
             }
             #pragma unroll
@@ -620,31 +607,25 @@
             lrun[r] = lrun[r] * alpha + ps;
             mrun[r] = mnew;
             #pragma unroll
-            for (int d = 0; d < 4; d++) oacc[d][r] *= alpha;
+            for (int d = 0; d < 4; d++) { o0[d][r] *= alpha; o1[d][r] *= alpha; }
             int prow = w*16 + lg*4 + r;
             #pragma unroll
             for (int ni = 0; ni < 2; ni++) {
-                unsigned short h,m,l; split3t(s[ni][r],h,m,l);
-                KP[0][prow*40 + ni*16 + lr] = h;
-                KP[1][prow*40 + ni*16 + lr] = m;
-                KP[2][prow*40 + ni*16 + lr] = l;
+                unsigned short hh2,mm2; split2h(sv[ni],hh2,mm2);
+                KP[0][prow*40 + ni*16 + lr] = hh2;
+                KP[1][prow*40 + ni*16 + lr] = mm2;
             }
         }
         {
-            bf16x8 ph = *(const bf16x8*)&KP[0][(w*16 + lr)*40 + lg*8];
-            bf16x8 pm = *(const bf16x8*)&KP[1][(w*16 + lr)*40 + lg*8];
-            bf16x8 pl = *(const bf16x8*)&KP[2][(w*16 + lr)*40 + lg*8];
+            f16x8 ph = *(const f16x8*)&KP[0][(w*16 + lr)*40 + lg*8];
+            f16x8 pm = *(const f16x8*)&KP[1][(w*16 + lr)*40 + lg*8];
             #pragma unroll
             for (int ni = 0; ni < 4; ni++) {
-                bf16x8 vh = *(const bf16x8*)&Vt[0][(ni*16 + lr)*40 + lg*8];
-                bf16x8 vm = *(const bf16x8*)&Vt[1][(ni*16 + lr)*40 + lg*8];
-                bf16x8 vl = *(const bf16x8*)&Vt[2][(ni*16 + lr)*40 + lg*8];
-                oacc[ni] = MFMA(ph, vh, oacc[ni]);
-                oacc[ni] = MFMA(ph, vm, oacc[ni]);
-                oacc[ni] = MFMA(pm, vh, oacc[ni]);
-                oacc[ni] = MFMA(ph, vl, oacc[ni]);
-                oacc[ni] = MFMA(pm, vm, oacc[ni]);
-                oacc[ni] = MFMA(pl, vh, oacc[ni]);
+                f16x8 vh = *(const f16x8*)&Vt[0][(ni*16 + lr)*40 + lg*8];
+                f16x8 vm = *(const f16x8*)&Vt[1][(ni*16 + lr)*40 + lg*8];
+                o0[ni] = MFMAH(ph, vh, o0[ni]);
+                o1[ni] = MFMAH(ph, vm, o1[ni]);
+                o1[ni] = MFMAH(pm, vh, o1[ni]);
             }
         }
         __syncthreads();
@@ -652,10 +633,11 @@
     float* obase = att + ((long)(b*SEQ + qt*64) * D_MODEL + hh*64);
     #pragma unroll
     for (int r = 0; r < 4; r++) {
-        float inv = 1.f / lrun[r];
+        float inv = DESCALE / lrun[r];
         #pragma unroll
         for (int ni = 0; ni < 4; ni++)
-            obase[(long)(w*16 + lg*4 + r) * D_MODEL + ni*16 + lr] = oacc[ni][r] * inv;
+            obase[(long)(w*16 + lg*4 + r) * D_MODEL + ni*16 + lr] =
+                (o0[ni][r] + o1[ni][r]*TIER) * inv;
     }
 }
 
@@ -684,22 +666,22 @@
             f32x4 vv = *(const f32x4*)(Bmat + (long)(n0+r)*D_MODEL + k0 + kc);
             u16x4 hv;
             #pragma unroll
-            for (int j = 0; j < 4; j++) hv[j] = f2bf(vv[j]);
+            for (int j = 0; j < 4; j++) hv[j] = f2h(vv[j]);
             *(u16x4*)&Bs[r*LDSS + kc] = hv;
         }
         __syncthreads();
-        bf16x8 bfv[4], af[4];
+        f16x8 bfv[4], af[4];
         #pragma unroll
         for (int ni = 0; ni < 4; ni++)
-            bfv[ni] = *(const bf16x8*)&Bs[(wn + ni*16 + lr)*LDSS + lg*8];
+            bfv[ni] = *(const f16x8*)&Bs[(wn + ni*16 + lr)*LDSS + lg*8];
         #pragma unroll
         for (int mi = 0; mi < 4; mi++)
-            af[mi] = *(const bf16x8*)&As[(wm + mi*16 + lr)*LDSS + lg*8];
+            af[mi] = *(const f16x8*)&As[(wm + mi*16 + lr)*LDSS + lg*8];
         #pragma unroll
         for (int mi = 0; mi < 4; mi++)
             #pragma unroll
             for (int ni = 0; ni < 4; ni++)
-                acc[mi][ni] = MFMA(af[mi], bfv[ni], acc[mi][ni]);
+                acc[mi][ni] = MFMAH(af[mi], bfv[ni], acc[mi][ni]);
         __syncthreads();
     }
     #pragma unroll
@@ -710,7 +692,7 @@
             #pragma unroll
             for (int ni = 0; ni < 4; ni++) {
                 int col = n0 + wn + ni*16 + lr;
-                C[row*VOCAB + col] = acc[mi][ni][r];
+                C[row*VOCAB + col] = acc[mi][ni][r] * INV_S;
             }
         }
 }
@@ -756,7 +738,7 @@
     kk[base+1] = kr*sn + ki*cs;
 }
 
-__global__ __launch_bounds__(64) void gate_kernel(const unsigned short* __restrict__ xf3,
+__global__ __launch_bounds__(64) void gate_kernel(const unsigned short* __restrict__ xf2,
     const float* __restrict__ gw, int* __restrict__ counts,
     int* __restrict__ eid, float* __restrict__ wts, float* __restrict__ pbuf)
 {
@@ -765,12 +747,11 @@
     float acc[8] = {0,0,0,0,0,0,0,0};
     for (int d0 = lane*4; d0 < D_MODEL; d0 += 256) {
         long idx = (long)n*D_MODEL + d0;
-        u16x4 xh = *(const u16x4*)(xf3 + 0*PSA + idx);
-        u16x4 xm = *(const u16x4*)(xf3 + 1*PSA + idx);
-        u16x4 xl = *(const u16x4*)(xf3 + 2*PSA + idx);
+        u16x4 xh = *(const u16x4*)(xf2 + 0*PSA + idx);
+        u16x4 xm = *(const u16x4*)(xf2 + 1*PSA + idx);
         #pragma unroll
         for (int j = 0; j < 4; j++) {
-            float xv = bf2f(xh[j]) + bf2f(xm[j]) + bf2f(xl[j]);
+            float xv = h2f(xh[j])*INV_S + h2f(xm[j])*INV_M;
             const float* g = gw + (d0+j) * 8;
             #pragma unroll
             for (int e = 0; e < 8; e++) acc[e] += xv * g[e];
@@ -822,9 +803,9 @@
     __syncthreads();
     if (t == 0) {
         int o = 0; float a = 0.f;
-        for (int k = 0; k < 8; k++) {
-            offs[k] = o; cursor[k] = o; o += counts[k];
-            a += (float)counts[k] * red[k];
+        for (int kk = 0; kk < 8; kk++) {
+            offs[kk] = o; cursor[kk] = o; o += counts[kk];
+            a += (float)counts[kk] * red[kk];
         }
         aux[0] += 8.f * a / ((float)NTOK * (float)NTOK);
     }
@@ -883,15 +864,15 @@
     float* pbuf   = (float*)(W + 4096 + 65536);
     float* rtab   = (float*)(W + 4096 + 131072 + 65536);
     float*          h    = (float*)(W + 1*MB);
-    unsigned short* hn3  = (unsigned short*)(W + 9*MB);
-    float*          qf   = (float*)(W + 21*MB);
-    float*          kf   = (float*)(W + 29*MB);
-    float*          vf   = (float*)(W + 37*MB);
-    unsigned short* wq3  = (unsigned short*)(W + 45*MB);
-    unsigned short* wk3  = (unsigned short*)(W + 51*MB);
-    unsigned short* wv3  = (unsigned short*)(W + 57*MB);
-    float*          att  = (float*)(W + 45*MB);
-    float*          g    = (float*)(W + 21*MB);
+    unsigned short* hn2  = (unsigned short*)(W + 9*MB);
+    float*          qf   = (float*)(W + 17*MB);
+    float*          kf   = (float*)(W + 25*MB);
+    float*          vf   = (float*)(W + 33*MB);
+    unsigned short* wq2  = (unsigned short*)(W + 41*MB);
+    unsigned short* wk2  = (unsigned short*)(W + 45*MB);
+    unsigned short* wv2  = (unsigned short*)(W + 49*MB);
+    float*          att  = (float*)(W + 41*MB);
+    float*          g    = (float*)(W + 17*MB);
 
     hipMemsetAsync(W, 0, 256, stream);
     ropetab_kernel<<<(SEQ*32 + 255)/256, 256, 0, stream>>>(rtab);
@@ -903,16 +884,16 @@
         const float* wvl = wv + (size_t)l*D_MODEL*D_MODEL;
         const float* wol = wo + (size_t)l*D_MODEL*D_MODEL;
 
-        rmsnorm_kernel<<<NTOK, 256, 0, stream>>>(h, anw + (size_t)l*D_MODEL, hn3);
-        wsplitT_kernel<<<dim3(16, 16, 3), 256, 0, stream>>>(wql, wkl, wvl, wq3, wk3, wv3);
-        qkv_kernel<<<dim3(D_MODEL/64, NTOK/64, 3), 256, 0, stream>>>(hn3, wq3, wk3, wv3, qf, kf, vf);
+        rmsnorm_kernel<<<NTOK, 256, 0, stream>>>(h, anw + (size_t)l*D_MODEL, hn2);
+        wsplitT_kernel<<<dim3(16, 16, 3), 256, 0, stream>>>(wql, wkl, wvl, wq2, wk2, wv2);
+        qkv_kernel<<<dim3(D_MODEL/64, NTOK/64, 3), 256, 0, stream>>>(hn2, wq2, wk2, wv2, qf, kf, vf);
         rope_kernel<<<(NTOK*512 + 255)/256, 256, 0, stream>>>(qf, kf, rtab);
         attn_kernel<<<dim3(SEQ/64, BATCH*NHEADS), 256, 0, stream>>>(qf, kf, vf, att);
         wo_kernel<<<dim3(D_MODEL/64, NTOK/64), 256, 0, stream>>>(att, wol, h);
 
-        rmsnorm_kernel<<<NTOK, 256, 0, stream>>>(h, fnw + (size_t)l*D_MODEL, hn3);
+        rmsnorm_kernel<<<NTOK, 256, 0, stream>>>(h, fnw + (size_t)l*D_MODEL, hn2);
         hipMemsetAsync(W, 0, 160, stream);
-        gate_kernel<<<NTOK, 64, 0, stream>>>(hn3, gw + (size_t)l*D_MODEL*NEXP, counts, eid, wts, pbuf);
+        gate_kernel<<<NTOK, 64, 0, stream>>>(hn2, gw + (size_t)l*D_MODEL*NEXP, counts, eid, wts, pbuf);
         scan_kernel<<<1, 64, 0, stream>>>(counts, offs, cursor, pbuf, aux);
         assign_kernel<<<(NTOK + 255)/256, 256, 0, stream>>>(eid, wts, cursor, rowix, wrow);
 
@@ -922,15 +903,15 @@
         dim3 g13(FFH/128, 2*NTOK/64, NEXP);
         dim3 g2d(D_MODEL/64, 2*NTOK/64, NEXP);
         if (l == 0) {
-            moe13_kernel<3><<<g13, 256, 0, stream>>>(hn3, w1l, w3l, g, rowix, counts, offs);
-            w2_kernel<3><<<g2d, 256, 0, stream>>>(g, w2l, h, rowix, wrow, counts, offs);
+            moe13_kernel<2><<<g13, 256, 0, stream>>>(hn2, w1l, w3l, g, rowix, counts, offs);
+            w2_kernel<2><<<g2d, 256, 0, stream>>>(g, w2l, h, rowix, wrow, counts, offs);
         } else {
-            moe13_kernel<1><<<g13, 256, 0, stream>>>(hn3, w1l, w3l, g, rowix, counts, offs);
+            moe13_kernel<1><<<g13, 256, 0, stream>>>(hn2, w1l, w3l, g, rowix, counts, offs);
             w2_kernel<1><<<g2d, 256, 0, stream>>>(g, w2l, h, rowix, wrow, counts, offs);
         }
     }
 
-    rmsnorm_kernel<<<NTOK, 256, 0, stream>>>(h, finw, hn3);
-    logits_kernel<<<dim3(NTOK/128, VOCAB/128), 256, 0, stream>>>(hn3, emb, out);
+    rmsnorm_kernel<<<NTOK, 256, 0, stream>>>(h, finw, hn2);
+    logits_kernel<<<dim3(NTOK/128, VOCAB/128), 256, 0, stream>>>(hn2, emb, out);
     write_aux_kernel<<<1, 1, 0, stream>>>(out, aux);
 }
```
